# Performance work log

Measured on AMD Instinct MI355X. Metric: run time of the kernel, lower is better.

Reference implementation:

```python
import jax, jax.numpy as jnp
import numpy as np

# CODABlocks (codomain attention) with per_channel_attention=True:
# token_codimension = head_codimension = 1, scale = 2, n_modes = [32, 32],
# mixer_modes = [16, 16], temperature = 1.0, instance_norm (affine) everywhere.
N_HEADS = 16
TEMPERATURE = 1.0
EPS = 1e-5

def _gelu(z):
    return jax.nn.gelu(z, approximate=False)  # matches torch F.gelu default (erf)

def instance_norm(x, g, b):
    # x: (B, C, H, W); normalize over spatial dims per (sample, channel), affine.
    mu = jnp.mean(x, axis=(-2, -1), keepdims=True)
    var = jnp.var(x, axis=(-2, -1), keepdims=True)
    return (x - mu) * jax.lax.rsqrt(var + EPS) * g[:, None, None] + b[:, None, None]

def conv1x1(x, w, b):
    return jnp.einsum('bihw,io->bohw', x, w) + b[None, :, None, None]

def fourier_resample(x, out_shape):
    # FFT-based spatial resampling (mode truncation / zero-pad), norm='forward'.
    if tuple(x.shape[-2:]) == tuple(out_shape):
        return x
    Ho, Wo = out_shape
    xft = jnp.fft.rfftn(x, axes=(-2, -1), norm='forward')
    out = jnp.zeros(x.shape[:-2] + (Ho, Wo // 2 + 1), dtype=xft.dtype)
    hk = min(x.shape[-2], Ho) // 2
    wk = min(xft.shape[-1], Wo // 2 + 1)
    out = out.at[..., :hk, :wk].set(xft[..., :hk, :wk])
    out = out.at[..., -hk:, :wk].set(xft[..., -hk:, :wk])
    return jnp.fft.irfftn(out, s=out_shape, axes=(-2, -1), norm='forward')

def spectral_conv(x, w, out_shape):
    # Truncated-mode spectral convolution (dense weights, equiv. to tucker rank=1.0).
    # w: (Cin, Cout, 2*mh, mw, 2) -> complex weight on kept Fourier modes.
    wc = w[..., 0] + 1j * w[..., 1]
    mh = wc.shape[2] // 2
    mw = wc.shape[3]
    Ho, Wo = out_shape
    xft = jnp.fft.rfftn(x, axes=(-2, -1), norm='forward')   # (B, Cin, H, W//2+1)
    top = jnp.einsum('bihw,iohw->bohw', xft[:, :, :mh, :mw], wc[:, :, :mh])
    bot = jnp.einsum('bihw,iohw->bohw', xft[:, :, -mh:, :mw], wc[:, :, mh:])
    out_ft = jnp.zeros((x.shape[0], wc.shape[1], Ho, Wo // 2 + 1), dtype=xft.dtype)
    out_ft = out_ft.at[:, :, :mh, :mw].set(top)
    out_ft = out_ft.at[:, :, -mh:, :mw].set(bot)
    return jnp.fft.irfftn(out_ft, s=out_shape, axes=(-2, -1), norm='forward')

def fno_layer(x, spec_w, skip_w, skip_b, out_shape, norm=None, act=None):
    # One FNOBlocks layer: spectral conv + (resampled) linear skip, optional norm/act.
    xs = fourier_resample(conv1x1(x, skip_w, skip_b), out_shape)
    xf = spectral_conv(x, spec_w, out_shape)
    if norm is not None:
        xf = instance_norm(xf, *norm)
    y = xf + xs
    return act(y) if act is not None else y

def codano_forward(x, key_w, key_skip_w, key_skip_b, query_w, query_skip_w, query_skip_b, value_w, value_skip_w, value_skip_b, proj_w, proj_skip_w, proj_skip_b, norm1_g, norm1_b, attn_norm_g, attn_norm_b, norm2_g, norm2_b, mixer_w1, mixer_skip_w1, mixer_skip_b1, mixer_norm_g1, mixer_norm_b1, mixer_w2, mixer_skip_w2, mixer_skip_b2, mixer_norm_g2, mixer_norm_b2, mixer_out_g, mixer_out_b):
    b, t, H, W = x.shape   # token codim d = 1 -> channel dim == number of tokens
    tokens = x.reshape(b * t, 1, H, W)
    tokens_norm = instance_norm(tokens, norm1_g, norm1_b)
    Hs, Ws = H // 2, W // 2   # K, Q downsampled by scale = 2
    k = fno_layer(tokens_norm, key_w, key_skip_w, key_skip_b, (Hs, Ws))
    q = fno_layer(tokens_norm, query_w, query_skip_w, query_skip_b, (Hs, Ws))
    v = fno_layer(tokens_norm, value_w, value_skip_w, value_skip_b, (H, W))

    def heads_flat(z):
        hh, ww = z.shape[-2:]
        # (b*t, n_heads*d, h, w) -> (b, heads, t, d*h*w), d = 1
        return z.reshape(b, t, N_HEADS, hh * ww).transpose(0, 2, 1, 3)

    kf, qf, vf = heads_flat(k), heads_flat(q), heads_flat(v)
    scale = jnp.sqrt(jnp.asarray(kf.shape[-1], jnp.float32)) * TEMPERATURE
    dprod = jax.nn.softmax(jnp.einsum('bhtd,bhsd->bhts', qf, kf) / scale, axis=-1)
    attn = jnp.einsum('bhts,bhsd->bhtd', dprod, vf)      # (b, heads, t, H*W)
    attn = attn.transpose(0, 2, 1, 3).reshape(b * t, N_HEADS, H, W)
    # multi-head projection back to token codimension (n_heads -> 1)
    attn = fno_layer(attn, proj_w, proj_skip_w, proj_skip_b, (H, W))
    attn = instance_norm(attn + tokens, attn_norm_g, attn_norm_b)
    # permutation-equivariant mixer: 2 FNO layers shared across all tokens
    m = instance_norm(attn, norm2_g, norm2_b)
    m = fno_layer(m, mixer_w1, mixer_skip_w1, mixer_skip_b1, (H, W), norm=(mixer_norm_g1, mixer_norm_b1), act=_gelu)
    m = fno_layer(m, mixer_w2, mixer_skip_w2, mixer_skip_b2, (H, W), norm=(mixer_norm_g2, mixer_norm_b2))
    out = instance_norm(m, mixer_out_g, mixer_out_b) + attn
    return out.reshape(b, t, H, W)

def setup_inputs():
    key = jax.random.key(0)
    ks = list(jax.random.split(key, 32))
    f32 = jnp.float32
    def W_(k, shape, s=0.02):
        return (s * jax.random.normal(k, shape)).astype(f32)
    B, T, H, Wd = 4, 32, 128, 128
    mh_s, mw_s = 16, 9    # mixer_modes [16,16]: 2*(16//2) rows, 16//2+1 rfft cols
    mh_f, mw_f = 32, 17   # n_modes [32,32]
    return {
        'x': jax.random.normal(ks[0], (B, T, H, Wd), dtype=f32),
        'key_w': W_(ks[1], (1, N_HEADS, mh_s, mw_s, 2)),
        'key_skip_w': W_(ks[2], (1, N_HEADS), 0.5),
        'key_skip_b': W_(ks[3], (N_HEADS,)),
        'query_w': W_(ks[4], (1, N_HEADS, mh_s, mw_s, 2)),
        'query_skip_w': W_(ks[5], (1, N_HEADS), 0.5),
        'query_skip_b': W_(ks[6], (N_HEADS,)),
        'value_w': W_(ks[7], (1, N_HEADS, mh_s, mw_s, 2)),
        'value_skip_w': W_(ks[8], (1, N_HEADS), 0.5),
        'value_skip_b': W_(ks[9], (N_HEADS,)),
        'proj_w': W_(ks[10], (N_HEADS, 1, mh_f, mw_f, 2)),
        'proj_skip_w': W_(ks[11], (N_HEADS, 1), 0.25),
        'proj_skip_b': W_(ks[12], (1,)),
        'norm1_g': jnp.ones((1,), f32), 'norm1_b': jnp.zeros((1,), f32),
        'attn_norm_g': jnp.ones((1,), f32), 'attn_norm_b': jnp.zeros((1,), f32),
        'norm2_g': jnp.ones((1,), f32), 'norm2_b': jnp.zeros((1,), f32),
        'mixer_w1': W_(ks[13], (1, 1, mh_f, mw_f, 2)),
        'mixer_skip_w1': W_(ks[14], (1, 1), 0.5),
        'mixer_skip_b1': W_(ks[15], (1,)),
        'mixer_norm_g1': jnp.ones((1,), f32), 'mixer_norm_b1': jnp.zeros((1,), f32),
        'mixer_w2': W_(ks[16], (1, 1, mh_f, mw_f, 2)),
        'mixer_skip_w2': W_(ks[17], (1, 1), 0.5),
        'mixer_skip_b2': W_(ks[18], (1,)),
        'mixer_norm_g2': jnp.ones((1,), f32), 'mixer_norm_b2': jnp.zeros((1,), f32),
        'mixer_out_g': jnp.ones((1,), f32), 'mixer_out_b': jnp.zeros((1,), f32),
    }

def reference(x, key_w, key_skip_w, key_skip_b, query_w, query_skip_w, query_skip_b, value_w, value_skip_w, value_skip_b, proj_w, proj_skip_w, proj_skip_b, norm1_g, norm1_b, attn_norm_g, attn_norm_b, norm2_g, norm2_b, mixer_w1, mixer_skip_w1, mixer_skip_b1, mixer_norm_g1, mixer_norm_b1, mixer_w2, mixer_skip_w2, mixer_skip_b2, mixer_norm_g2, mixer_norm_b2, mixer_out_g, mixer_out_b):
    return codano_forward(x, key_w, key_skip_w, key_skip_b, query_w, query_skip_w, query_skip_b, value_w, value_skip_w, value_skip_b, proj_w, proj_skip_w, proj_skip_b, norm1_g, norm1_b, attn_norm_g, attn_norm_b, norm2_g, norm2_b, mixer_w1, mixer_skip_w1, mixer_skip_b1, mixer_norm_g1, mixer_norm_b1, mixer_w2, mixer_skip_w2, mixer_skip_b2, mixer_norm_g2, mixer_norm_b2, mixer_out_g, mixer_out_b)
```

## Files before the change

### kernel.cpp

```cpp
#include <hip/hip_runtime.h>
#include <cmath>

#define PI_F 3.14159265358979323846f
#define NTOK 128
#define NPIX 16384
#define NHEADS 16

__device__ __forceinline__ void block_reduce2(float& a, float& b){
  __shared__ float sa[4], sb[4];
  __syncthreads();
  for (int o=32;o>0;o>>=1){ a += __shfl_down(a,o); b += __shfl_down(b,o); }
  int w = threadIdx.x>>6, l = threadIdx.x&63;
  if (l==0){ sa[w]=a; sb[w]=b; }
  __syncthreads();
  a = sa[0]+sa[1]+sa[2]+sa[3];
  b = sb[0]+sb[1]+sb[2]+sb[3];
}

__device__ __forceinline__ float block_reduce1(float a){
  __shared__ float sa[4];
  __syncthreads();
  for (int o=32;o>0;o>>=1) a += __shfl_down(a,o);
  int w = threadIdx.x>>6, l = threadIdx.x&63;
  if (l==0) sa[w]=a;
  __syncthreads();
  return sa[0]+sa[1]+sa[2]+sa[3];
}

__device__ __forceinline__ float gelu_f(float y){
  return 0.5f*y*(1.f + erff(y*0.70710678118f));
}

__device__ __forceinline__ void affine_from(const float* __restrict__ ps, float g, float bb, int t,
                                            float& a, float& b0){
  float sum=0.f,sq=0.f;
  #pragma unroll
  for (int s=0;s<8;s++){ const float* p=ps+((size_t)t*8+s)*2; sum+=p[0]; sq+=p[1]; }
  const float iN=1.f/NPIX;
  float mu=sum*iN, var=sq*iN-mu*mu;
  a=rsqrtf(var+1e-5f)*g;
  b0=bb-mu*a;
}
__device__ __forceinline__ void scalA_from(const float* __restrict__ psA, float ag, float n2g, int t,
                                           float& muZ, float& aA, float& a0){
  float sum=0.f,sq=0.f;
  #pragma unroll
  for (int s=0;s<16;s++){ const float* p=psA+((size_t)t*16+s)*2; sum+=p[0]; sq+=p[1]; }
  const float iN=1.f/NPIX;
  muZ=sum*iN; float var=sq*iN-muZ*muZ;
  float inv=rsqrtf(var+1e-5f);
  aA=inv*ag;
  float var2=aA*aA*var;
  a0=aA*rsqrtf(var2+1e-5f)*n2g;
}
__device__ __forceinline__ void scalB_from(const float* __restrict__ psB, float mng1, int t,
                                           float& mu1, float& c1){
  float sum=0.f,sq=0.f;
  #pragma unroll
  for (int s=0;s<16;s++){ const float* p=psB+((size_t)t*16+s)*2; sum+=p[0]; sq+=p[1]; }
  const float iN=1.f/NPIX;
  mu1=sum*iN; float var=sq*iN-mu1*mu1;
  c1=rsqrtf(var+1e-5f)*mng1;
}
__device__ __forceinline__ void scalC_from(const float* __restrict__ psC, float mng2, float K, float sw,
                                           float outg, int t,
                                           float& mu2f, float& c2, float& mu3, float& c3){
  float sf=0.f,sfsq=0.f,sm=0.f,smsq=0.f,sx=0.f;
  #pragma unroll
  for (int s=0;s<16;s++){
    const float* p=psC+((size_t)t*16+s)*5;
    sf+=p[0]; sfsq+=p[1]; sm+=p[2]; smsq+=p[3]; sx+=p[4];
  }
  const float iN=1.f/NPIX;
  mu2f=sf*iN; float var2=sfsq*iN-mu2f*mu2f;
  c2=rsqrtf(var2+1e-5f)*mng2;
  float Em1=sm*iN, Em1sq=smsq*iN, Exm=sx*iN;
  float Em2=K+sw*Em1;
  float Em2sq = c2*c2*var2 + sw*sw*Em1sq + K*K
              + 2.f*c2*sw*(Exm - mu2f*Em1) + 2.f*K*sw*Em1;
  float var_m2=Em2sq-Em2*Em2;
  mu3=Em2;
  c3=rsqrtf(var_m2+1e-5f)*outg;
}

__global__ __launch_bounds__(256) void k_scol(const float* __restrict__ x,
                        float* __restrict__ A, float* __restrict__ pstat){
  int bx=blockIdx.x;
  if (bx<1024){
    __shared__ float rows[2048];
    __shared__ float S1[2592];
    __shared__ float tw[256];
    int base = bx*16;
    for (int i=threadIdx.x;i<2048;i+=256) rows[i] = x[(size_t)base*128 + i];
    for (int p=threadIdx.x;p<128;p+=256){ float sn,cs; sincosf(-(2.f*PI_F/128.f)*(float)p,&sn,&cs); tw[p*2]=cs; tw[p*2+1]=sn; }
    __syncthreads();
    for (int e=threadIdx.x;e<1280;e+=256){
      int r=e/80, q=e%80, w0=q/5, k=q%5;
      const float* y=rows+r*128+w0;
      float re=0.f, im=0.f;
      #pragma unroll
      for (int w1=0;w1<8;w1++){
        int p=(16*k*w1)&127;
        float v=y[w1*16];
        re+=v*tw[p*2]; im+=v*tw[p*2+1];
      }
      float* o=S1+r*162+q*2; o[0]=re; o[1]=im;
    }
    __syncthreads();
    for (int e=threadIdx.x;e<528;e+=256){
      int r=e/33, c=e%33;
      int m=c&7; int ks=m; float sg=1.f;
      if (m>4){ ks=8-m; sg=-1.f; }
      const float* Sp=S1+r*162+ks*2;
      float re=0.f, im=0.f;
      #pragma unroll
      for (int w0=0;w0<16;w0++){
        int p=(c*w0)&127;
        float cr=tw[p*2], ci=tw[p*2+1];
        float sr=Sp[w0*10], si=sg*Sp[w0*10+1];
        re += sr*cr - si*ci;
        im += sr*ci + si*cr;
      }
      float* o=A+((size_t)(base+r)*33+c)*2; o[0]=re; o[1]=im;
    }
  } else {
    int u=bx-1024; int t=u>>3, slab=u&7;
    const float* xs = x + (size_t)t*NPIX + slab*2048;
    float sum=0.f, sq=0.f;
    for (int i=threadIdx.x;i<2048;i+=256){ float v=xs[i]; sum+=v; sq+=v*v; }
    block_reduce2(sum,sq);
    if (threadIdx.x==0){ float* o=pstat+((size_t)t*8+slab)*2; o[0]=sum; o[1]=sq; }
  }
}

__global__ __launch_bounds__(256) void k_rowfft64(const float* __restrict__ A,
                          const float* __restrict__ pstat0,
                          const float* __restrict__ n1g, const float* __restrict__ n1b,
                          float* __restrict__ X64, float* __restrict__ X64h){
  int s=blockIdx.x, cg2=blockIdx.y;
  int c0=cg2*11;
  __shared__ float a[128*11*2];
  __shared__ float S1[11*290];
  __shared__ float S[64][11][2];
  __shared__ float tw[128][2];
  for (int i=threadIdx.x;i<128*22;i+=256){
    int r=i/22, q=i%22;
    a[(r*11+(q>>1))*2+(q&1)] = A[((size_t)(s*128+r)*33 + c0)*2 + q];
  }
  for (int p=threadIdx.x;p<128;p+=256){ float sn,cs; sincosf(-(2.f*PI_F/128.f)*(float)p,&sn,&cs); tw[p][0]=cs; tw[p][1]=sn; }
  float af,b0; affine_from(pstat0, n1g[0], n1b[0], s, af, b0);
  __syncthreads();
  for (int e=threadIdx.x;e<1408;e+=256){
    int cl=e>>7, q=e&127, h0=q>>3, k=q&7;
    float re=0.f, im=0.f;
    #pragma unroll
    for (int h1=0;h1<8;h1++){
      int p=(16*k*h1)&127;
      float cr=tw[p][0], ci=tw[p][1];
      const float* ap=a+((h0+16*h1)*11+cl)*2;
      float ar=ap[0], ai=ap[1];
      re += ar*cr - ai*ci;
      im += ar*ci + ai*cr;
    }
    float* o=S1+cl*290+h0*18+k*2; o[0]=re; o[1]=im;
  }
  __syncthreads();
  const float sc=1.f/16384.f;
  for (int e=threadIdx.x;e<64*11;e+=256){
    int i2=e/11, cl=e%11;
    int r=(i2<32)? i2 : i2+64;
    int k=r&7;
    const float* Sp=S1+cl*290+k*2;
    float re=0.f, im=0.f;
    #pragma unroll
    for (int h0=0;h0<16;h0++){
      int p=(r*h0)&127;
      float cr=tw[p][0], ci=tw[p][1];
      float sr=Sp[h0*18], si=Sp[h0*18+1];
      re += sr*cr - si*ci;
      im += sr*ci + si*cr;
    }
    float vr = af*re*sc, vi = af*im*sc;
    if (r==0 && (c0+cl)==0) vr += b0;
    S[i2][cl][0]=vr; S[i2][cl][1]=vi;
  }
  __syncthreads();
  for (int e=threadIdx.x;e<64*11;e+=256){
    int r=e/11, cl=e%11; int c=c0+cl;
    float vr=S[r][cl][0], vi=S[r][cl][1];
    float* o=X64+((size_t)s*(64*33)+r*33+c)*2; o[0]=vr; o[1]=vi;
    float hr=vr, hi=vi;
    if (c==0 || c==32){
      int pr=(64-r)&63;
      hr=0.5f*(vr+S[pr][cl][0]);
      hi=0.5f*(vi-S[pr][cl][1]);
    }
    float* oh=X64h+((size_t)s*(64*33)+r*33+c)*2; oh[0]=hr; oh[1]=hi;
  }
}

__global__ __launch_bounds__(256) void k_UeZYw(const float* __restrict__ X64, const float* __restrict__ X64h,
    const float* __restrict__ qw, const float* __restrict__ qsw,
    const float* __restrict__ kw, const float* __restrict__ ksw,
    const float* __restrict__ value_w, const float* __restrict__ vsw, const float* __restrict__ vsb,
    const float* __restrict__ proj_w, const float* __restrict__ psw,
    float* __restrict__ Zq, float* __restrict__ Zk, float* __restrict__ Yw,
    float* __restrict__ Ue){
  __shared__ float sh[4224];
  int bx=blockIdx.x;
  if (bx<2048){
    int t=bx>>4, h=bx&15;
    float* Xs = sh;
    float2* xh0 = (float2*)(sh+1092);
    for (int e=threadIdx.x;e<544;e+=256){
      int j=e/17, c=e%17;
      int i2=(j<16)? j : (j+32);
      const float* xp = X64 + ((size_t)t*(64*33) + i2*33 + c)*2;
      Xs[e*2]=xp[0]; Xs[e*2+1]=xp[1];
    }
    if (threadIdx.x<17){
      int j=threadIdx.x;
      int r=(j<=8)? j : j+47;
      const float* hp = X64h + ((size_t)t*(64*33) + r*33)*2;
      xh0[j]=make_float2(hp[0],hp[1]);
    }
    __syncthreads();
    float aq=qsw[h], ak=ksw[h];
    for (int e=threadIdx.x;e<306;e+=256){
      int side=e/153, m=e%153;
      int j=m/9, c=m%9;
      int jj=(j<=8)? j : j+15;
      const float* W = side? kw : qw;
      float a = side? ak : aq;
      float prx=0.f, pry=0.f;
      if (j!=8){
        int jw=(j<8)? j : j-1;
        const float* wp = W + ((size_t)(h*16+jw)*9 + c)*2;
        float xrr=Xs[(jj*17+c)*2], xri=Xs[(jj*17+c)*2+1];
        prx = wp[0]*xrr - wp[1]*xri;
        pry = wp[0]*xri + wp[1]*xrr;
      }
      float Vx=prx, Vy=pry;
      if (c==0){
        int jp = (j==0)? 0 : 17-j;
        float ppx=0.f, ppy=0.f;
        if (jp!=8){
          int jw2=(jp<8)? jp : jp-1;
          const float* wp2 = W + ((size_t)(h*16+jw2)*9)*2;
          int jj2=(jp<=8)? jp : jp+15;
          float x2r=Xs[(jj2*17)*2], x2i=Xs[(jj2*17)*2+1];
          ppx = wp2[0]*x2r - wp2[1]*x2i;
          ppy = wp2[0]*x2i + wp2[1]*x2r;
        }
        Vx = 0.5f*(prx + ppx);
        Vy = 0.5f*(pry - ppy);
      }
      float xmr, xmi;
      if (c==0){ xmr=xh0[j].x; xmi=xh0[j].y; }
      else { xmr=Xs[(jj*17+c)*2]; xmi=Xs[(jj*17+c)*2+1]; }
      float zr = a*xmr + Vx;
      float zi = a*xmi + Vy;
      float wf = (side && c!=0)? 2.f : 1.f;
      float* dst = (side? Zk : Zq) + ((size_t)(t*16+h))*306 + m*2;
      dst[0]=wf*zr; dst[1]=wf*zi;
    }
    int b=t>>5, s=t&31;
    float vw=vsw[h], vb=vsb[h], pw=psw[h];
    size_t obase = ((size_t)(b*16+h)*32 + s)*1088;
    for (int e=threadIdx.x;e<544;e+=256){
      int j=e/17, c=e%17;
      float xr=Xs[e*2], xi=Xs[e*2+1];
      float wvr=0.f,wvi=0.f;
      if (c<=8 && (j<8||j>=24)){
        int jw=(j<8)? j : (j-16);
        const float* wv = value_w + ((size_t)(h*16+jw)*9 + c)*2;
        wvr=wv[0]; wvi=wv[1];
      }
      float Mr=xr*wvr-xi*wvi, Mi=xr*wvi+xi*wvr;
      float Mhr=Mr, Mhi=Mi;
      if (c==0){
        float Pr2=0.f,Pi2=0.f;
        int jp2=(j==0)?0:((j==16)?-1:32-j);
        if (jp2>=0 && (jp2<8||jp2>=24)){
          int jw2=(jp2<8)? jp2 : (jp2-16);
          const float* wv2=value_w+((size_t)(h*16+jw2)*9)*2;
          float pxr=Xs[(jp2*17)*2], pxi=Xs[(jp2*17)*2+1];
          Pr2=pxr*wv2[0]-pxi*wv2[1];
          Pi2=pxr*wv2[1]+pxi*wv2[0];
        }
        Mhr=0.5f*(Mr+Pr2); Mhi=0.5f*(Mi-Pi2);
      }
      float Yr=vw*xr+Mhr+((e==0)? vb:0.f);
      float Yi=vw*xi+Mhi;
      const float* pc=proj_w+((size_t)(h*32+j)*17+c)*2;
      float pr=pc[0], pi=pc[1];
      float* o=Yw+obase+e*2;
      o[0]=pr*Yr-pi*Yi+pw*Mr;
      o[1]=pr*Yi+pi*Yr+pw*Mi;
    }
  } else {
    int u=bx-2048;
    int b=u>>8, rem=u&255, t=rem>>3, sg=rem&7;
    float2* xt=(float2*)sh;
    const float2* src = (const float2*)(X64h + ((size_t)(b*32+t))*4224);
    for (int m=threadIdx.x;m<2112;m+=256){
      int r=m/33, c=m%33;
      bool excl = (c<=8) && (r<=8 || r>=56);
      float w = excl? 0.f : ((c==0||c==32)? 1.f : 2.f);
      float2 v = src[m];
      xt[m]=make_float2(v.x*w, v.y*w);
    }
    __syncthreads();
    float acc[4]={0.f,0.f,0.f,0.f};
    const float2* s0=(const float2*)(X64h + ((size_t)(b*32+sg*4))*4224);
    for (int m=threadIdx.x;m<2112;m+=256){
      float2 a2=xt[m];
      #pragma unroll
      for (int j=0;j<4;j++){
        float2 b2=s0[(size_t)j*2112+m];
        acc[j]+=a2.x*b2.x+a2.y*b2.y;
      }
    }
    for (int j=0;j<4;j++){
      float r=block_reduce1(acc[j]);
      if (threadIdx.x==0) Ue[((size_t)(b*32+t))*32 + sg*4+j]=r;
    }
  }
}

__global__ __launch_bounds__(256) void k_scores2(const float* __restrict__ Zq, const float* __restrict__ Zk,
                          const float* __restrict__ Ue,
                          const float* __restrict__ qsw, const float* __restrict__ qsb,
                          const float* __restrict__ ksw, const float* __restrict__ ksb,
                          float* __restrict__ P){
  int b=blockIdx.x, h=blockIdx.y, tz=blockIdx.z;
  __shared__ float2 zq[16][154];
  __shared__ float2 zk[16][154];
  __shared__ float Pl[16][33];
  for (int i=threadIdx.x;i<16*153;i+=256){
    int t=i/153, m=i%153;
    zq[t][m]=((const float2*)(Zq + ((size_t)((b*32+tz*16+t)*16+h))*306))[m];
  }
  float aq=qsw[h], ak=ksw[h], bq=qsb[h], bk=ksb[h];
  float aqak=aq*ak;
  int tl=threadIdx.x>>4, sl=threadIdx.x&15;
  for (int ch=0; ch<2; ch++){
    __syncthreads();
    for (int i=threadIdx.x;i<16*153;i+=256){
      int s=i/153, m=i%153;
      zk[s][m]=((const float2*)(Zk + ((size_t)((b*32+ch*16+s)*16+h))*306))[m];
    }
    __syncthreads();
    float acc=0.f;
    for (int m=0;m<153;m++){
      float2 a2=zq[tl][m], c2=zk[sl][m];
      acc += a2.x*c2.x + a2.y*c2.y;
    }
    int s=ch*16+sl;
    float G = aqak*Ue[((size_t)(b*32+tz*16+tl))*32+s] + acc;
    Pl[tl][s] = 64.f*(G + bk*zq[tl][0].x + bq*zk[sl][0].x + bq*bk);
  }
  __syncthreads();
  if (threadIdx.x<16){
    int tt=threadIdx.x;
    float mx=-INFINITY;
    for (int s=0;s<32;s++) mx=fmaxf(mx,Pl[tt][s]);
    float e[32]; float sum=0.f;
    for (int s=0;s<32;s++){ e[s]=expf(Pl[tt][s]-mx); sum+=e[s]; }
    float inv=1.f/sum;
    size_t base=((size_t)(b*16+h)*32+tz*16+tt)*32;
    for (int s=0;s<32;s++) P[base+s]=e[s]*inv;
  }
}

__global__ __launch_bounds__(256) void k_SfSk(const float* __restrict__ x, const float* __restrict__ P,
        const float* __restrict__ Yw,
        const float* __restrict__ pw, const float* __restrict__ vw,
        const float* __restrict__ pstat0, const float* __restrict__ n1g, const float* __restrict__ n1b,
        float* __restrict__ Sfp, float* __restrict__ sk){
  __shared__ float sh[4096];
  int bx=blockIdx.x;
  if (bx<272){
    int b=bx/68, rem=bx%68, ec=rem/4, g=rem%4;
    int e0=ec*64, hs0=g*128;
    float (*Pl)[32] = (float(*)[32])sh;
    for (int i=threadIdx.x;i<128*32;i+=256){
      int hsl=i>>5, t=i&31;
      int hs=hs0+hsl, h=hs>>5, s=hs&31;
      Pl[hsl][t]=P[(((size_t)(b*16+h)*32)+t)*32+s];
    }
    __syncthreads();
    int el=threadIdx.x&63, tg=threadIdx.x>>6;
    float acc[8];
    #pragma unroll
    for (int j=0;j<8;j++) acc[j]=0.f;
    const float* Yb = Yw + ((size_t)b*512 + hs0)*1088 + e0 + el;
    #pragma unroll 4
    for (int hsl=0;hsl<128;hsl++){
      float y = Yb[(size_t)hsl*1088];
      #pragma unroll
      for (int j=0;j<8;j++) acc[j] += Pl[hsl][tg*8+j]*y;
    }
    #pragma unroll
    for (int j=0;j<8;j++){
      int t=tg*8+j;
      Sfp[((size_t)(b*32+t)*4+g)*1088 + e0 + el] = acc[j];
    }
  } else {
    int u=bx-272;
    int b=u>>6, rem=u&63, ch=rem>>1, tt=rem&1;
    int pxb=ch*512;
    float* Rs = sh;
    float* cbs = sh+512;
    float* as2 = sh+528;
    float* b0s = sh+560;
    if (threadIdx.x<32){
      float a,b0; affine_from(pstat0, n1g[0], n1b[0], b*32+threadIdx.x, a, b0);
      as2[threadIdx.x]=a; b0s[threadIdx.x]=b0;
    }
    __syncthreads();
    for (int rr=threadIdx.x; rr<512; rr+=256){
      int tl=rr>>5, s=rr&31;
      int t=tt*16+tl;
      float acc=0.f;
      for (int h=0;h<16;h++)
        acc += pw[h]*vw[h]*P[(((size_t)(b*16+h)*32)+t)*32+s];
      Rs[tl*32+s]=acc*as2[s];
      float cb=acc*b0s[s];
      for (int o=16;o>0;o>>=1) cb+=__shfl_down(cb,o,32);
      if (s==0) cbs[tl]=cb;
    }
    __syncthreads();
    float a0[16], a1[16];
    #pragma unroll
    for (int t=0;t<16;t++){ a0[t]=0.f; a1[t]=0.f; }
    for (int s=0;s<32;s++){
      const float* xp = x + ((size_t)(b*32+s))*NPIX + pxb;
      float v0=xp[threadIdx.x], v1=xp[threadIdx.x+256];
      #pragma unroll
      for (int t=0;t<16;t++){ float r=Rs[t*32+s]; a0[t]+=r*v0; a1[t]+=r*v1; }
    }
    #pragma unroll
    for (int t=0;t<16;t++){
      int gt=tt*16+t;
      float cb=cbs[t];
      float* op = sk + ((size_t)(b*32+gt))*NPIX + pxb;
      op[threadIdx.x]=a0[t]+cb; op[threadIdx.x+256]=a1[t]+cb;
    }
  }
}

__global__ __launch_bounds__(256) void k_f0sp(const float* __restrict__ Sfp,
        const float* __restrict__ sk, const float* __restrict__ x,
        const float* __restrict__ P, const float* __restrict__ X64,
        const float* __restrict__ pstat0,
        const float* __restrict__ n1g, const float* __restrict__ n1b,
        const float* __restrict__ pw, const float* __restrict__ vw,
        const float* __restrict__ psw, const float* __restrict__ vsb, const float* __restrict__ psb,
        float* __restrict__ zf, float* __restrict__ pstatA, float* __restrict__ sp){
  __shared__ float sh[1616];
  int bx=blockIdx.x;
  if (bx<2048){
    int bt=bx>>4, slab=bx&15;
    float* Ss=sh; float* T=sh+1088; float* tw=sh+1360;
    for (int i=threadIdx.x;i<1088;i+=256){
      const float* sp4 = Sfp + (size_t)bt*4352 + i;
      Ss[i] = sp4[0]+sp4[1088]+sp4[2176]+sp4[3264];
    }
    for (int p=threadIdx.x;p<128;p+=256){ float sn,cs; sincosf((2.f*PI_F/128.f)*(float)p,&sn,&cs); tw[p*2]=cs; tw[p*2+1]=sn; }
    __syncthreads();
    int h0 = slab*8;
    for (int e=threadIdx.x;e<136;e+=256){
      int hl=e/17, c=e%17; int h=h0+hl;
      float re=0.f, im=0.f;
      for (int j=0;j<32;j++){
        int r=(j<16)? j : (j+96);
        int p=(r*h)&127;
        float cs=tw[p*2], sn=tw[p*2+1];
        float ar=Ss[(j*17+c)*2], ai=Ss[(j*17+c)*2+1];
        re += ar*cs - ai*sn;
        im += ar*sn + ai*cs;
      }
      T[e*2]=re; T[e*2+1]=im;
    }
    __syncthreads();
    size_t base = (size_t)bt*NPIX + h0*128;
    float Cb = psb[0];
    for (int hh=0;hh<16;hh++) Cb += psw[hh]*vsb[hh];
    int w=threadIdx.x&127, hl0=threadIdx.x>>7;
    float cw[16], swt[16];
    #pragma unroll
    for (int c=0;c<16;c++){ int p=((c+1)*w)&127; cw[c]=tw[p*2]; swt[c]=tw[p*2+1]; }
    float sum=0.f, sq=0.f;
    #pragma unroll
    for (int pp=0;pp<4;pp++){
      int hl=hl0+2*pp;
      const float2* Th=(const float2*)(T+hl*34);
      float v=Th[0].x;
      #pragma unroll
      for (int c=0;c<16;c++){ float2 th=Th[c+1]; v += 2.f*(th.x*cw[c] - th.y*swt[c]); }
      int pos=hl*128+w;
      float val = v + sk[base+pos] + x[base+pos] + Cb;
      zf[base+pos]=val; sum+=val; sq+=val*val;
    }
    block_reduce2(sum,sq);
    if (threadIdx.x==0){ float* o=pstatA+((size_t)bt*16+slab)*2; o[0]=sum; o[1]=sq; }
  } else {
    int u=bx-2048;
    int bt=u>>1, ec=u&1; int b=bt>>5, t=bt&31;
    float* Sfl=sh; float* Rs=sh+1088;
    if (threadIdx.x<32){
      int s=threadIdx.x; float acc=0.f;
      for (int h=0;h<16;h++)
        acc += pw[h]*vw[h]*P[(((size_t)(b*16+h)*32)+t)*32+s];
      Rs[s]=acc;
    }
    for (int i=threadIdx.x;i<1088;i+=256){
      const float* sp4 = Sfp + (size_t)bt*4352 + i;
      Sfl[i]=sp4[0]+sp4[1088]+sp4[2176]+sp4[3264];
    }
    __syncthreads();
    float a_t,b0_t; affine_from(pstat0,n1g[0],n1b[0],bt,a_t,b0_t);
    float Cb=psb[0];
    for (int h=0;h<16;h++) Cb+=psw[h]*vsb[h];
    float inva=1.f/a_t;
    int e1=ec*272, e2=e1+272;
    for (int e=e1+threadIdx.x;e<e2;e+=256){
      int j=e/17, c=e%17;
      float sr=Sfl[e*2], si=Sfl[e*2+1];
      if (c==0){
        if (j==0){ si=0.f; }
        else if (j==16){ sr*=0.5f; si*=0.5f; }
        else { int jp=32-j; sr=0.5f*(sr+Sfl[jp*34]); si=0.5f*(si-Sfl[jp*34+1]); }
      }
      int i2=(j<16)? j : (j+32);
      float re=0.f, im=0.f;
      const float* xb = X64 + ((size_t)(b*32)*(64*33) + i2*33 + c)*2;
      for (int s=0;s<32;s++){
        const float* xp = xb + (size_t)s*(64*33)*2;
        float r=Rs[s];
        re += r*xp[0]; im += r*xp[1];
      }
      const float* xt = X64 + ((size_t)bt*(64*33) + i2*33 + c)*2;
      re += inva*xt[0]; im += inva*xt[1];
      float zr=sr+re, zi=si+im;
      if (e==0) zr += Cb - b0_t*inva;
      sp[((size_t)bt*544+e)*2]=zr; sp[((size_t)bt*544+e)*2+1]=zi;
    }
  }
}

__global__ __launch_bounds__(256) void k_field1(const float* __restrict__ sp, const float* __restrict__ wm,
        const float* __restrict__ pstatA,
        const float* __restrict__ ag, const float* __restrict__ n2g, const float* __restrict__ n2b,
        float* __restrict__ fd1, float* __restrict__ pstatB){
  int bt = blockIdx.x, slab = blockIdx.y;
  __shared__ float Ss[1088];
  __shared__ float T[8*17*2];
  __shared__ float tw[128][2];
  float muZ,aA,a0;
  scalA_from(pstatA, ag[0], n2g[0], bt, muZ, aA, a0);
  float d0 = n2b[0] - muZ*a0;
  for (int e=threadIdx.x;e<544;e+=256){
    float xr=a0*sp[((size_t)bt*544+e)*2] + ((e==0)? d0 : 0.f);
    float xi=a0*sp[((size_t)bt*544+e)*2+1];
    float wr=wm[e*2], wi=wm[e*2+1];
    Ss[e*2]=xr*wr-xi*wi; Ss[e*2+1]=xr*wi+xi*wr;
  }
  for (int p=threadIdx.x;p<128;p+=256){ float sn,cs; sincosf((2.f*PI_F/128.f)*(float)p,&sn,&cs); tw[p][0]=cs; tw[p][1]=sn; }
  __syncthreads();
  int h0 = slab*8;
  for (int e=threadIdx.x;e<8*17;e+=256){
    int hl=e/17, c=e%17; int h=h0+hl;
    float re=0.f, im=0.f;
    for (int j=0;j<32;j++){
      int r=(j<16)? j : (j+96);
      int p=(r*h)&127;
      float cs=tw[p][0], sn=tw[p][1];
      float ar=Ss[(j*17+c)*2], ai=Ss[(j*17+c)*2+1];
      re += ar*cs - ai*sn;
      im += ar*sn + ai*cs;
    }
    T[e*2]=re; T[e*2+1]=im;
  }
  __syncthreads();
  size_t base = (size_t)bt*NPIX + h0*128;
  int w=threadIdx.x&127, hl0=threadIdx.x>>7;
  float cw[16], swt[16];
  #pragma unroll
  for (int c=0;c<16;c++){ int p=((c+1)*w)&127; cw[c]=tw[p][0]; swt[c]=tw[p][1]; }
  float sum=0.f, sq=0.f;
  #pragma unroll
  for (int pp=0;pp<4;pp++){
    int hl=hl0+2*pp;
    const float2* Th=(const float2*)(T+hl*34);
    float v=Th[0].x;
    #pragma unroll
    for (int c=0;c<16;c++){ float2 th=Th[c+1]; v += 2.f*(th.x*cw[c] - th.y*swt[c]); }
    int pos=hl*128+w;
    fd1[base+pos]=v; sum+=v; sq+=v*v;
  }
  block_reduce2(sum,sq);
  if (threadIdx.x==0){ float* o=pstatB+((size_t)bt*16+slab)*2; o[0]=sum; o[1]=sq; }
}

__global__ __launch_bounds__(256) void k_colA1(const float* __restrict__ f1, const float* __restrict__ z,
        const float* __restrict__ pstatA, const float* __restrict__ pstatB,
        const float* __restrict__ ag, const float* __restrict__ n2g, const float* __restrict__ mng1,
        const float* __restrict__ n2b,
        const float* __restrict__ mnb1, const float* __restrict__ msw1, const float* __restrict__ msb1,
        float* __restrict__ A){
  __shared__ float rows[16*128];
  __shared__ float S1[2592];
  __shared__ float tw[128][2];
  int grow = blockIdx.x*16;
  int t = grow>>7;
  float muZ,aA,a0;
  scalA_from(pstatA, ag[0], n2g[0], t, muZ, aA, a0);
  float b2 = n2b[0];
  float mu1,c1;
  scalB_from(pstatB, mng1[0], t, mu1, c1);
  float nb=mnb1[0], sw=msw1[0], sb=msb1[0];
  for (int i=threadIdx.x;i<2048;i+=256){
    size_t gi=(size_t)grow*128+i;
    float m0v=(z[gi]-muZ)*a0+b2;
    float y=(f1[gi]-mu1)*c1+nb + m0v*sw + sb;
    rows[i]=gelu_f(y);
  }
  for (int p=threadIdx.x;p<128;p+=256){ float sn,cs; sincosf(-(2.f*PI_F/128.f)*(float)p,&sn,&cs); tw[p][0]=cs; tw[p][1]=sn; }
  __syncthreads();
  for (int e=threadIdx.x;e<1280;e+=256){
    int r=e/80, q=e%80, w0=q/5, k=q%5;
    const float* y=rows+r*128+w0;
    float re=0.f, im=0.f;
    #pragma unroll
    for (int w1=0;w1<8;w1++){
      int p=(16*k*w1)&127;
      float v=y[w1*16];
      re+=v*tw[p][0]; im+=v*tw[p][1];
    }
    float* o=S1+r*162+q*2; o[0]=re; o[1]=im;
  }
  __syncthreads();
  for (int e=threadIdx.x;e<272;e+=256){
    int r=e/17, c=e%17;
    int m=c&7; int ks=m; float sg=1.f;
    if (m>4){ ks=8-m; sg=-1.f; }
    const float* Sp=S1+r*162+ks*2;
    float re=0.f, im=0.f;
    #pragma unroll
    for (int w0=0;w0<16;w0++){
      int p=(c*w0)&127;
      float cr=tw[p][0], ci=tw[p][1];
      float sr=Sp[w0*10], si=sg*Sp[w0*10+1];
      re += sr*cr - si*ci;
      im += sr*ci + si*cr;
    }
    float* o=A+((size_t)(grow+r)*17+c)*2; o[0]=re; o[1]=im;
  }
}

__global__ __launch_bounds__(256) void k_rowfft32(const float* __restrict__ A, float* __restrict__ spec){
  int s=blockIdx.x, cg2=blockIdx.y;
  int c0 = (cg2==0)? 0 : (1+cg2*4);
  int nc = (cg2==0)? 5 : 4;
  __shared__ float a[128*5*2];
  __shared__ float S1[5*290];
  __shared__ float tw[128][2];
  for (int i=threadIdx.x;i<128*nc*2;i+=256){
    int r=i/(2*nc), q=i%(2*nc);
    a[(r*5+(q>>1))*2+(q&1)] = A[((size_t)(s*128+r)*17 + c0)*2 + q];
  }
  for (int p=threadIdx.x;p<128;p+=256){ float sn,cs; sincosf(-(2.f*PI_F/128.f)*(float)p,&sn,&cs); tw[p][0]=cs; tw[p][1]=sn; }
  __syncthreads();
  for (int e=threadIdx.x;e<nc*128;e+=256){
    int cl=e>>7, q=e&127, h0=q>>3, k=q&7;
    float re=0.f, im=0.f;
    #pragma unroll
    for (int h1=0;h1<8;h1++){
      int p=(16*k*h1)&127;
      float cr=tw[p][0], ci=tw[p][1];
      const float* ap=a+((h0+16*h1)*5+cl)*2;
      float ar=ap[0], ai=ap[1];
      re += ar*cr - ai*ci;
      im += ar*ci + ai*cr;
    }
    float* o=S1+cl*290+h0*18+k*2; o[0]=re; o[1]=im;
  }
  __syncthreads();
  const float sc=1.f/16384.f;
  for (int e=threadIdx.x;e<32*nc;e+=256){
    int j=e/nc, cl=e%nc;
    int r=(j<16)? j : (j+96);
    int k=r&7;
    const float* Sp=S1+cl*290+k*2;
    float re=0.f,im=0.f;
    #pragma unroll
    for (int h0=0;h0<16;h0++){
      int p=(r*h0)&127;
      float cr=tw[p][0], ci=tw[p][1];
      float sr=Sp[h0*18], si=Sp[h0*18+1];
      re += sr*cr - si*ci;
      im += sr*ci + si*cr;
    }
    float* o=spec+((size_t)s*544 + j*17 + c0+cl)*2;
    o[0]=re*sc; o[1]=im*sc;
  }
}

__global__ __launch_bounds__(256) void k_field2(const float* __restrict__ sp2, const float* __restrict__ wm,
        const float* __restrict__ f1, const float* __restrict__ z,
        const float* __restrict__ pstatA, const float* __restrict__ pstatB,
        const float* __restrict__ ag, const float* __restrict__ n2g, const float* __restrict__ mng1,
        const float* __restrict__ n2b, const float* __restrict__ mnb1,
        const float* __restrict__ msw1, const float* __restrict__ msb1,
        float* __restrict__ fd2, float* __restrict__ pstatC){
  int bt = blockIdx.x, slab = blockIdx.y;
  __shared__ float Ss[1088];
  __shared__ float T[8*17*2];
  __shared__ float tw[128][2];
  for (int e=threadIdx.x;e<544;e+=256){
    float xr=sp2[((size_t)bt*544+e)*2], xi=sp2[((size_t)bt*544+e)*2+1];
    float wr=wm[e*2], wi=wm[e*2+1];
    Ss[e*2]=xr*wr-xi*wi; Ss[e*2+1]=xr*wi+xi*wr;
  }
  for (int p=threadIdx.x;p<128;p+=256){ float sn,cs; sincosf((2.f*PI_F/128.f)*(float)p,&sn,&cs); tw[p][0]=cs; tw[p][1]=sn; }
  __syncthreads();
  int h0 = slab*8;
  for (int e=threadIdx.x;e<8*17;e+=256){
    int hl=e/17, c=e%17; int h=h0+hl;
    float re=0.f, im=0.f;
    for (int j=0;j<32;j++){
      int r=(j<16)? j : (j+96);
      int p=(r*h)&127;
      float cs=tw[p][0], sn=tw[p][1];
      float ar=Ss[(j*17+c)*2], ai=Ss[(j*17+c)*2+1];
      re += ar*cs - ai*sn;
      im += ar*sn + ai*cs;
    }
    T[e*2]=re; T[e*2+1]=im;
  }
  __syncthreads();
  size_t base = (size_t)bt*NPIX + h0*128;
  float muZ,aA,a0,mu1,c1;
  scalA_from(pstatA, ag[0], n2g[0], bt, muZ, aA, a0);
  scalB_from(pstatB, mng1[0], bt, mu1, c1);
  float b2=n2b[0], nb1=mnb1[0], sw1=msw1[0], sb1=msb1[0];
  int w=threadIdx.x&127, hl0=threadIdx.x>>7;
  float cw[16], swt[16];
  #pragma unroll
  for (int c=0;c<16;c++){ int p=((c+1)*w)&127; cw[c]=tw[p][0]; swt[c]=tw[p][1]; }
  float s_f=0.f,s_fsq=0.f,s_m=0.f,s_msq=0.f,s_x=0.f;
  #pragma unroll
  for (int pp=0;pp<4;pp++){
    int hl=hl0+2*pp;
    const float2* Th=(const float2*)(T+hl*34);
    float v=Th[0].x;
    #pragma unroll
    for (int c=0;c<16;c++){ float2 th=Th[c+1]; v += 2.f*(th.x*cw[c] - th.y*swt[c]); }
    int pos=hl*128+w;
    size_t gi=base+pos;
    float m0v=(z[gi]-muZ)*a0+b2;
    float y=(f1[gi]-mu1)*c1+nb1 + m0v*sw1 + sb1;
    float m1v=gelu_f(y);
    fd2[gi]=v;
    s_f+=v; s_fsq+=v*v; s_m+=m1v; s_msq+=m1v*m1v; s_x+=v*m1v;
  }
  block_reduce2(s_f,s_fsq);
  block_reduce2(s_m,s_msq);
  s_x = block_reduce1(s_x);
  if (threadIdx.x==0){
    float* o=pstatC+((size_t)bt*16+slab)*5;
    o[0]=s_f; o[1]=s_fsq; o[2]=s_m; o[3]=s_msq; o[4]=s_x;
  }
}

__global__ __launch_bounds__(256) void k_final2(const float* __restrict__ z, const float* __restrict__ f1,
        const float* __restrict__ f2,
        const float* __restrict__ pstatA, const float* __restrict__ pstatB, const float* __restrict__ pstatC,
        const float* __restrict__ ag, const float* __restrict__ n2g, const float* __restrict__ mng1,
        const float* __restrict__ mng2, const float* __restrict__ outg,
        const float* __restrict__ ab, const float* __restrict__ n2b,
        const float* __restrict__ mnb1, const float* __restrict__ msw1, const float* __restrict__ msb1,
        const float* __restrict__ mnb2, const float* __restrict__ msw2, const float* __restrict__ msb2,
        const float* __restrict__ outb, float* __restrict__ out){
  int bt=blockIdx.x, slab=blockIdx.y;
  float muZ,aA,a0,mu1,c1,mu2f,c2,mu3,c3;
  scalA_from(pstatA, ag[0], n2g[0], bt, muZ, aA, a0);
  scalB_from(pstatB, mng1[0], bt, mu1, c1);
  float sw2=msw2[0], K=mnb2[0]+msb2[0];
  scalC_from(pstatC, mng2[0], K, sw2, outg[0], bt, mu2f, c2, mu3, c3);
  float b1=ab[0], b2=n2b[0], nb1=mnb1[0], sw1=msw1[0], sb1=msb1[0];
  float nb2=mnb2[0], sb2=msb2[0], bo=outb[0];
  size_t base=(size_t)bt*NPIX + (size_t)slab*1024;
  for (int i=threadIdx.x;i<1024;i+=256){
    size_t gi=base+i;
    float zv=z[gi];
    float m0v=(zv-muZ)*a0+b2;
    float a2v=(zv-muZ)*aA+b1;
    float y=(f1[gi]-mu1)*c1+nb1 + m0v*sw1 + sb1;
    float m1v=gelu_f(y);
    float m2v=(f2[gi]-mu2f)*c2+nb2 + m1v*sw2 + sb2;
    out[gi]=(m2v-mu3)*c3+bo+a2v;
  }
}

extern "C" void kernel_launch(void* const* d_in, const int* in_sizes, int n_in,
                              void* d_out, int out_size, void* d_ws, size_t ws_size,
                              hipStream_t stream){
  const float* x        = (const float*)d_in[0];
  const float* key_w    = (const float*)d_in[1];
  const float* key_sw   = (const float*)d_in[2];
  const float* key_sb   = (const float*)d_in[3];
  const float* query_w  = (const float*)d_in[4];
  const float* query_sw = (const float*)d_in[5];
  const float* query_sb = (const float*)d_in[6];
  const float* value_w  = (const float*)d_in[7];
  const float* value_sw = (const float*)d_in[8];
  const float* value_sb = (const float*)d_in[9];
  const float* proj_w   = (const float*)d_in[10];
  const float* proj_sw  = (const float*)d_in[11];
  const float* proj_sb  = (const float*)d_in[12];
  const float* norm1_g  = (const float*)d_in[13];
  const float* norm1_b  = (const float*)d_in[14];
  const float* attn_g   = (const float*)d_in[15];
  const float* attn_b   = (const float*)d_in[16];
  const float* norm2_g  = (const float*)d_in[17];
  const float* norm2_b  = (const float*)d_in[18];
  const float* mw1      = (const float*)d_in[19];
  const float* msw1     = (const float*)d_in[20];
  const float* msb1     = (const float*)d_in[21];
  const float* mng1     = (const float*)d_in[22];
  const float* mnb1     = (const float*)d_in[23];
  const float* mw2      = (const float*)d_in[24];
  const float* msw2     = (const float*)d_in[25];
  const float* msb2     = (const float*)d_in[26];
  const float* mng2     = (const float*)d_in[27];
  const float* mnb2     = (const float*)d_in[28];
  const float* outg     = (const float*)d_in[29];
  const float* outb     = (const float*)d_in[30];
  float* out = (float*)d_out;
  float* ws  = (float*)d_ws;

  size_t off=0;
  float* A   = ws + off; off += (size_t)128*128*33*2;
  float* X64 = ws + off; off += (size_t)128*64*33*2;
  float* X64h= ws + off; off += (size_t)128*64*33*2;
  float* Zq  = ws + off; off += (size_t)128*16*306;
  float* Zk  = ws + off; off += (size_t)128*16*306;
  float* Ue  = ws + off; off += (size_t)4*32*32;
  float* P   = ws + off; off += (size_t)4*16*32*32;
  float* Yw  = ws + off; off += (size_t)2048*1088;
  float* Sfp = ws + off; off += (size_t)128*4*1088;
  float* sk  = ws + off; off += (size_t)128*16384;
  float* zf  = ws + off; off += (size_t)128*16384;
  float* fd1 = ws + off; off += (size_t)128*16384;
  float* fd2 = ws + off; off += (size_t)128*16384;
  float* sp  = ws + off; off += (size_t)128*544*2;
  float* sp2 = ws + off; off += (size_t)128*544*2;
  float* pstat0 = ws + off; off += (size_t)128*8*2;
  float* pstatA = ws + off; off += (size_t)128*16*2;
  float* pstatB = ws + off; off += (size_t)128*16*2;
  float* pstatC = ws + off; off += (size_t)128*16*5;

  k_scol<<<2048,256,0,stream>>>(x, A, pstat0);
  k_rowfft64<<<dim3(128,3),256,0,stream>>>(A, pstat0, norm1_g, norm1_b, X64, X64h);
  k_UeZYw<<<3072,256,0,stream>>>(X64, X64h, query_w, query_sw, key_w, key_sw,
      value_w, value_sw, value_sb, proj_w, proj_sw, Zq, Zk, Yw, Ue);
  k_scores2<<<dim3(4,16,2),256,0,stream>>>(Zq, Zk, Ue, query_sw, query_sb, key_sw, key_sb, P);
  k_SfSk<<<528,256,0,stream>>>(x, P, Yw, proj_sw, value_sw, pstat0, norm1_g, norm1_b, Sfp, sk);
  k_f0sp<<<2304,256,0,stream>>>(Sfp, sk, x, P, X64, pstat0, norm1_g, norm1_b,
      proj_sw, value_sw, proj_sw, value_sb, proj_sb, zf, pstatA, sp);
  k_field1<<<dim3(128,16),256,0,stream>>>(sp, mw1, pstatA, attn_g, norm2_g, norm2_b, fd1, pstatB);
  k_colA1<<<1024,256,0,stream>>>(fd1, zf, pstatA, pstatB, attn_g, norm2_g, mng1,
      norm2_b, mnb1, msw1, msb1, A);
  k_rowfft32<<<dim3(128,4),256,0,stream>>>(A, sp2);
  k_field2<<<dim3(128,16),256,0,stream>>>(sp2, mw2, fd1, zf, pstatA, pstatB,
      attn_g, norm2_g, mng1, norm2_b, mnb1, msw1, msb1, fd2, pstatC);
  k_final2<<<dim3(128,16),256,0,stream>>>(zf, fd1, fd2, pstatA, pstatB, pstatC,
      attn_g, norm2_g, mng1, mng2, outg, attn_b, norm2_b,
      mnb1, msw1, msb1, mnb2, msw2, msb2, outb, out);
}
```

Before: 271.7 us.

## Fuse all stages into one persistent megakernel with grid-wide barriers

Turns each of the eleven kernels into device functions and runs them inside one persistent kernel of 1024 blocks, separated by atomic-counter grid barriers. This removes per-kernel launch overhead and the drain/fill gaps between dependent stages. The occupancy query guards against deadlock by falling back to the old multi-kernel path. The score stage also changes its key chunking from 2x16 to 4x8, leaving half the threads idle in the dot-product loop. The cost is that barrier spinning and stages with fewer blocks than the grid leave part of the machine idle, plus the loss of __restrict__ hints.

```diff
diff --git a/kernel.cpp b/kernel.cpp
--- a/kernel.cpp
+++ b/kernel.cpp
@@ -5,6 +5,7 @@
 #define NTOK 128
 #define NPIX 16384
 #define NHEADS 16
+#define NBLK 1024u
 
 __device__ __forceinline__ void block_reduce2(float& a, float& b){
   __shared__ float sa[4], sb[4];
@@ -31,7 +32,19 @@
   return 0.5f*y*(1.f + erff(y*0.70710678118f));
 }
 
-__device__ __forceinline__ void affine_from(const float* __restrict__ ps, float g, float bb, int t,
+__device__ __forceinline__ void gbar(unsigned* cnt){
+  __syncthreads();
+  __threadfence();
+  if (threadIdx.x==0){
+    atomicAdd(cnt, 1u);
+    while (__hip_atomic_load(cnt, __ATOMIC_RELAXED, __HIP_MEMORY_SCOPE_AGENT) < NBLK)
+      __builtin_amdgcn_s_sleep(2);
+  }
+  __syncthreads();
+  __threadfence();
+}
+
+__device__ __forceinline__ void affine_from(const float* ps, float g, float bb, int t,
                                             float& a, float& b0){
   float sum=0.f,sq=0.f;
   #pragma unroll
@@ -41,7 +54,7 @@
   a=rsqrtf(var+1e-5f)*g;
   b0=bb-mu*a;
 }
-__device__ __forceinline__ void scalA_from(const float* __restrict__ psA, float ag, float n2g, int t,
+__device__ __forceinline__ void scalA_from(const float* psA, float ag, float n2g, int t,
                                            float& muZ, float& aA, float& a0){
   float sum=0.f,sq=0.f;
   #pragma unroll
@@ -53,7 +66,7 @@
   float var2=aA*aA*var;
   a0=aA*rsqrtf(var2+1e-5f)*n2g;
 }
-__device__ __forceinline__ void scalB_from(const float* __restrict__ psB, float mng1, int t,
+__device__ __forceinline__ void scalB_from(const float* psB, float mng1, int t,
                                            float& mu1, float& c1){
   float sum=0.f,sq=0.f;
   #pragma unroll
@@ -62,7 +75,7 @@
   mu1=sum*iN; float var=sq*iN-mu1*mu1;
   c1=rsqrtf(var+1e-5f)*mng1;
 }
-__device__ __forceinline__ void scalC_from(const float* __restrict__ psC, float mng2, float K, float sw,
+__device__ __forceinline__ void scalC_from(const float* psC, float mng2, float K, float sw,
                                            float outg, int t,
                                            float& mu2f, float& c2, float& mu3, float& c3){
   float sf=0.f,sfsq=0.f,sm=0.f,smsq=0.f,sx=0.f;
@@ -83,16 +96,14 @@
   c3=rsqrtf(var_m2+1e-5f)*outg;
 }
 
-__global__ __launch_bounds__(256) void k_scol(const float* __restrict__ x,
-                        float* __restrict__ A, float* __restrict__ pstat){
-  int bx=blockIdx.x;
+
+__device__ __forceinline__ void st_scol(int bx, float* sh, const float* x,
+                                        float* A, float* pstat){
   if (bx<1024){
-    __shared__ float rows[2048];
-    __shared__ float S1[2592];
-    __shared__ float tw[256];
+    float* rows=sh; float* S1=sh+2048; float* tw=sh+4640;
     int base = bx*16;
     for (int i=threadIdx.x;i<2048;i+=256) rows[i] = x[(size_t)base*128 + i];
-    for (int p=threadIdx.x;p<128;p+=256){ float sn,cs; sincosf(-(2.f*PI_F/128.f)*(float)p,&sn,&cs); tw[p*2]=cs; tw[p*2+1]=sn; }
+    for (int q=threadIdx.x;q<128;q+=256){ float sn,cs; sincosf(-(2.f*PI_F/128.f)*(float)q,&sn,&cs); tw[q*2]=cs; tw[q*2+1]=sn; }
     __syncthreads();
     for (int e=threadIdx.x;e<1280;e+=256){
       int r=e/80, q=e%80, w0=q/5, k=q%5;
@@ -133,21 +144,20 @@
   }
 }
 
-__global__ __launch_bounds__(256) void k_rowfft64(const float* __restrict__ A,
-                          const float* __restrict__ pstat0,
-                          const float* __restrict__ n1g, const float* __restrict__ n1b,
-                          float* __restrict__ X64, float* __restrict__ X64h){
-  int s=blockIdx.x, cg2=blockIdx.y;
+__device__ __forceinline__ void st_row64(int u, float* sh, const float* A,
+                          const float* pstat0, const float* n1g, const float* n1b,
+                          float* X64, float* X64h){
+  int s=u%128, cg2=u/128;
   int c0=cg2*11;
-  __shared__ float a[128*11*2];
-  __shared__ float S1[11*290];
-  __shared__ float S[64][11][2];
-  __shared__ float tw[128][2];
+  float* a=sh;
+  float* S1=sh+2816;
+  float* S=sh+6006;
+  float* tw=sh+7414;
   for (int i=threadIdx.x;i<128*22;i+=256){
     int r=i/22, q=i%22;
     a[(r*11+(q>>1))*2+(q&1)] = A[((size_t)(s*128+r)*33 + c0)*2 + q];
   }
-  for (int p=threadIdx.x;p<128;p+=256){ float sn,cs; sincosf(-(2.f*PI_F/128.f)*(float)p,&sn,&cs); tw[p][0]=cs; tw[p][1]=sn; }
+  for (int q=threadIdx.x;q<128;q+=256){ float sn,cs; sincosf(-(2.f*PI_F/128.f)*(float)q,&sn,&cs); tw[q*2]=cs; tw[q*2+1]=sn; }
   float af,b0; affine_from(pstat0, n1g[0], n1b[0], s, af, b0);
   __syncthreads();
   for (int e=threadIdx.x;e<1408;e+=256){
@@ -156,7 +166,7 @@
     #pragma unroll
     for (int h1=0;h1<8;h1++){
       int p=(16*k*h1)&127;
-      float cr=tw[p][0], ci=tw[p][1];
+      float cr=tw[p*2], ci=tw[p*2+1];
       const float* ap=a+((h0+16*h1)*11+cl)*2;
       float ar=ap[0], ai=ap[1];
       re += ar*cr - ai*ci;
@@ -175,39 +185,35 @@
     #pragma unroll
     for (int h0=0;h0<16;h0++){
       int p=(r*h0)&127;
-      float cr=tw[p][0], ci=tw[p][1];
+      float cr=tw[p*2], ci=tw[p*2+1];
       float sr=Sp[h0*18], si=Sp[h0*18+1];
       re += sr*cr - si*ci;
       im += sr*ci + si*cr;
     }
     float vr = af*re*sc, vi = af*im*sc;
     if (r==0 && (c0+cl)==0) vr += b0;
-    S[i2][cl][0]=vr; S[i2][cl][1]=vi;
+    S[(i2*11+cl)*2]=vr; S[(i2*11+cl)*2+1]=vi;
   }
   __syncthreads();
   for (int e=threadIdx.x;e<64*11;e+=256){
     int r=e/11, cl=e%11; int c=c0+cl;
-    float vr=S[r][cl][0], vi=S[r][cl][1];
+    float vr=S[(r*11+cl)*2], vi=S[(r*11+cl)*2+1];
     float* o=X64+((size_t)s*(64*33)+r*33+c)*2; o[0]=vr; o[1]=vi;
     float hr=vr, hi=vi;
     if (c==0 || c==32){
       int pr=(64-r)&63;
-      hr=0.5f*(vr+S[pr][cl][0]);
-      hi=0.5f*(vi-S[pr][cl][1]);
+      hr=0.5f*(vr+S[(pr*11+cl)*2]);
+      hi=0.5f*(vi-S[(pr*11+cl)*2+1]);
     }
     float* oh=X64h+((size_t)s*(64*33)+r*33+c)*2; oh[0]=hr; oh[1]=hi;
   }
 }
 
-__global__ __launch_bounds__(256) void k_UeZYw(const float* __restrict__ X64, const float* __restrict__ X64h,
-    const float* __restrict__ qw, const float* __restrict__ qsw,
-    const float* __restrict__ kw, const float* __restrict__ ksw,
-    const float* __restrict__ value_w, const float* __restrict__ vsw, const float* __restrict__ vsb,
-    const float* __restrict__ proj_w, const float* __restrict__ psw,
-    float* __restrict__ Zq, float* __restrict__ Zk, float* __restrict__ Yw,
-    float* __restrict__ Ue){
-  __shared__ float sh[4224];
-  int bx=blockIdx.x;
+__device__ __forceinline__ void st_uezyw(int bx, float* sh, const float* X64, const float* X64h,
+    const float* qw, const float* qsw, const float* kw, const float* ksw,
+    const float* value_w, const float* vsw, const float* vsb,
+    const float* proj_w, const float* psw,
+    float* Zq, float* Zk, float* Yw, float* Ue){
   if (bx<2048){
     int t=bx>>4, h=bx&15;
     float* Xs = sh;
@@ -265,7 +271,7 @@
       dst[0]=wf*zr; dst[1]=wf*zi;
     }
     int b=t>>5, s=t&31;
-    float vw=vsw[h], vb=vsb[h], pw=psw[h];
+    float vw_=vsw[h], vb=vsb[h], pw=psw[h];
     size_t obase = ((size_t)(b*16+h)*32 + s)*1088;
     for (int e=threadIdx.x;e<544;e+=256){
       int j=e/17, c=e%17;
@@ -290,8 +296,8 @@
         }
         Mhr=0.5f*(Mr+Pr2); Mhi=0.5f*(Mi-Pi2);
       }
-      float Yr=vw*xr+Mhr+((e==0)? vb:0.f);
-      float Yi=vw*xi+Mhi;
+      float Yr=vw_*xr+Mhr+((e==0)? vb:0.f);
+      float Yi=vw_*xi+Mhi;
       const float* pc=proj_w+((size_t)(h*32+j)*17+c)*2;
       float pr=pc[0], pi=pc[1];
       float* o=Yw+obase+e*2;
@@ -328,58 +334,55 @@
   }
 }
 
-__global__ __launch_bounds__(256) void k_scores2(const float* __restrict__ Zq, const float* __restrict__ Zk,
-                          const float* __restrict__ Ue,
-                          const float* __restrict__ qsw, const float* __restrict__ qsb,
-                          const float* __restrict__ ksw, const float* __restrict__ ksb,
-                          float* __restrict__ P){
-  int b=blockIdx.x, h=blockIdx.y, tz=blockIdx.z;
-  __shared__ float2 zq[16][154];
-  __shared__ float2 zk[16][154];
-  __shared__ float Pl[16][33];
+__device__ __forceinline__ void st_scores(int u, float* sh, const float* Zq, const float* Zk,
+                          const float* Ue, const float* qsw, const float* qsb,
+                          const float* ksw, const float* ksb, float* P){
+  int b=u&3, h=(u>>2)&15, tz=u>>6;
+  float2* zq=(float2*)sh;
+  float2* zk=(float2*)(sh+4928);
+  float*  Pl=sh+7392;
   for (int i=threadIdx.x;i<16*153;i+=256){
     int t=i/153, m=i%153;
-    zq[t][m]=((const float2*)(Zq + ((size_t)((b*32+tz*16+t)*16+h))*306))[m];
+    zq[t*154+m]=((const float2*)(Zq + ((size_t)((b*32+tz*16+t)*16+h))*306))[m];
   }
   float aq=qsw[h], ak=ksw[h], bq=qsb[h], bk=ksb[h];
   float aqak=aq*ak;
   int tl=threadIdx.x>>4, sl=threadIdx.x&15;
-  for (int ch=0; ch<2; ch++){
-    __syncthreads();
-    for (int i=threadIdx.x;i<16*153;i+=256){
+  for (int ch=0; ch<4; ch++){
+    __syncthreads();
+    for (int i=threadIdx.x;i<8*153;i+=256){
       int s=i/153, m=i%153;
-      zk[s][m]=((const float2*)(Zk + ((size_t)((b*32+ch*16+s)*16+h))*306))[m];
-    }
-    __syncthreads();
-    float acc=0.f;
-    for (int m=0;m<153;m++){
-      float2 a2=zq[tl][m], c2=zk[sl][m];
-      acc += a2.x*c2.x + a2.y*c2.y;
-    }
-    int s=ch*16+sl;
-    float G = aqak*Ue[((size_t)(b*32+tz*16+tl))*32+s] + acc;
-    Pl[tl][s] = 64.f*(G + bk*zq[tl][0].x + bq*zk[sl][0].x + bq*bk);
+      zk[s*154+m]=((const float2*)(Zk + ((size_t)((b*32+ch*8+s)*16+h))*306))[m];
+    }
+    __syncthreads();
+    if (sl<8){
+      float acc=0.f;
+      for (int m=0;m<153;m++){
+        float2 a2=zq[tl*154+m], c2=zk[sl*154+m];
+        acc += a2.x*c2.x + a2.y*c2.y;
+      }
+      int s=ch*8+sl;
+      float G = aqak*Ue[((size_t)(b*32+tz*16+tl))*32+s] + acc;
+      Pl[tl*32+s] = 64.f*(G + bk*zq[tl*154].x + bq*zk[sl*154].x + bq*bk);
+    }
   }
   __syncthreads();
   if (threadIdx.x<16){
     int tt=threadIdx.x;
     float mx=-INFINITY;
-    for (int s=0;s<32;s++) mx=fmaxf(mx,Pl[tt][s]);
+    for (int s=0;s<32;s++) mx=fmaxf(mx,Pl[tt*32+s]);
     float e[32]; float sum=0.f;
-    for (int s=0;s<32;s++){ e[s]=expf(Pl[tt][s]-mx); sum+=e[s]; }
+    for (int s=0;s<32;s++){ e[s]=expf(Pl[tt*32+s]-mx); sum+=e[s]; }
     float inv=1.f/sum;
     size_t base=((size_t)(b*16+h)*32+tz*16+tt)*32;
     for (int s=0;s<32;s++) P[base+s]=e[s]*inv;
   }
 }
 
-__global__ __launch_bounds__(256) void k_SfSk(const float* __restrict__ x, const float* __restrict__ P,
-        const float* __restrict__ Yw,
-        const float* __restrict__ pw, const float* __restrict__ vw,
-        const float* __restrict__ pstat0, const float* __restrict__ n1g, const float* __restrict__ n1b,
-        float* __restrict__ Sfp, float* __restrict__ sk){
-  __shared__ float sh[4096];
-  int bx=blockIdx.x;
+__device__ __forceinline__ void st_sfsk(int bx, float* sh, const float* x, const float* P,
+        const float* Yw, const float* pw, const float* vw,
+        const float* pstat0, const float* n1g, const float* n1b,
+        float* Sfp, float* sk){
   if (bx<272){
     int b=bx/68, rem=bx%68, ec=rem/4, g=rem%4;
     int e0=ec*64, hs0=g*128;
@@ -450,16 +453,12 @@
   }
 }
 
-__global__ __launch_bounds__(256) void k_f0sp(const float* __restrict__ Sfp,
-        const float* __restrict__ sk, const float* __restrict__ x,
-        const float* __restrict__ P, const float* __restrict__ X64,
-        const float* __restrict__ pstat0,
-        const float* __restrict__ n1g, const float* __restrict__ n1b,
-        const float* __restrict__ pw, const float* __restrict__ vw,
-        const float* __restrict__ psw, const float* __restrict__ vsb, const float* __restrict__ psb,
-        float* __restrict__ zf, float* __restrict__ pstatA, float* __restrict__ sp){
-  __shared__ float sh[1616];
-  int bx=blockIdx.x;
+__device__ __forceinline__ void st_f0sp(int bx, float* sh, const float* Sfp,
+        const float* sk, const float* x, const float* P, const float* X64,
+        const float* pstat0, const float* n1g, const float* n1b,
+        const float* pw, const float* vw,
+        const float* psw, const float* vsb, const float* psb,
+        float* zf, float* pstatA, float* sp){
   if (bx<2048){
     int bt=bx>>4, slab=bx&15;
     float* Ss=sh; float* T=sh+1088; float* tw=sh+1360;
@@ -467,7 +466,7 @@
       const float* sp4 = Sfp + (size_t)bt*4352 + i;
       Ss[i] = sp4[0]+sp4[1088]+sp4[2176]+sp4[3264];
     }
-    for (int p=threadIdx.x;p<128;p+=256){ float sn,cs; sincosf((2.f*PI_F/128.f)*(float)p,&sn,&cs); tw[p*2]=cs; tw[p*2+1]=sn; }
+    for (int q=threadIdx.x;q<128;q+=256){ float sn,cs; sincosf((2.f*PI_F/128.f)*(float)q,&sn,&cs); tw[q*2]=cs; tw[q*2+1]=sn; }
     __syncthreads();
     int h0 = slab*8;
     for (int e=threadIdx.x;e<136;e+=256){
@@ -550,14 +549,11 @@
   }
 }
 
-__global__ __launch_bounds__(256) void k_field1(const float* __restrict__ sp, const float* __restrict__ wm,
-        const float* __restrict__ pstatA,
-        const float* __restrict__ ag, const float* __restrict__ n2g, const float* __restrict__ n2b,
-        float* __restrict__ fd1, float* __restrict__ pstatB){
-  int bt = blockIdx.x, slab = blockIdx.y;
-  __shared__ float Ss[1088];
-  __shared__ float T[8*17*2];
-  __shared__ float tw[128][2];
+__device__ __forceinline__ void st_field1(int u, float* sh, const float* sp, const float* wm,
+        const float* pstatA, const float* ag, const float* n2g, const float* n2b,
+        float* fd1, float* pstatB){
+  int bt=u&127, slab=u>>7;
+  float* Ss=sh; float* T=sh+1088; float* tw=sh+1360;
   float muZ,aA,a0;
   scalA_from(pstatA, ag[0], n2g[0], bt, muZ, aA, a0);
   float d0 = n2b[0] - muZ*a0;
@@ -567,7 +563,7 @@
     float wr=wm[e*2], wi=wm[e*2+1];
     Ss[e*2]=xr*wr-xi*wi; Ss[e*2+1]=xr*wi+xi*wr;
   }
-  for (int p=threadIdx.x;p<128;p+=256){ float sn,cs; sincosf((2.f*PI_F/128.f)*(float)p,&sn,&cs); tw[p][0]=cs; tw[p][1]=sn; }
+  for (int q=threadIdx.x;q<128;q+=256){ float sn,cs; sincosf((2.f*PI_F/128.f)*(float)q,&sn,&cs); tw[q*2]=cs; tw[q*2+1]=sn; }
   __syncthreads();
   int h0 = slab*8;
   for (int e=threadIdx.x;e<8*17;e+=256){
@@ -576,7 +572,7 @@
     for (int j=0;j<32;j++){
       int r=(j<16)? j : (j+96);
       int p=(r*h)&127;
-      float cs=tw[p][0], sn=tw[p][1];
+      float cs=tw[p*2], sn=tw[p*2+1];
       float ar=Ss[(j*17+c)*2], ai=Ss[(j*17+c)*2+1];
       re += ar*cs - ai*sn;
       im += ar*sn + ai*cs;
@@ -588,7 +584,7 @@
   int w=threadIdx.x&127, hl0=threadIdx.x>>7;
   float cw[16], swt[16];
   #pragma unroll
-  for (int c=0;c<16;c++){ int p=((c+1)*w)&127; cw[c]=tw[p][0]; swt[c]=tw[p][1]; }
+  for (int c=0;c<16;c++){ int p=((c+1)*w)&127; cw[c]=tw[p*2]; swt[c]=tw[p*2+1]; }
   float sum=0.f, sq=0.f;
   #pragma unroll
   for (int pp=0;pp<4;pp++){
@@ -604,16 +600,12 @@
   if (threadIdx.x==0){ float* o=pstatB+((size_t)bt*16+slab)*2; o[0]=sum; o[1]=sq; }
 }
 
-__global__ __launch_bounds__(256) void k_colA1(const float* __restrict__ f1, const float* __restrict__ z,
-        const float* __restrict__ pstatA, const float* __restrict__ pstatB,
-        const float* __restrict__ ag, const float* __restrict__ n2g, const float* __restrict__ mng1,
-        const float* __restrict__ n2b,
-        const float* __restrict__ mnb1, const float* __restrict__ msw1, const float* __restrict__ msb1,
-        float* __restrict__ A){
-  __shared__ float rows[16*128];
-  __shared__ float S1[2592];
-  __shared__ float tw[128][2];
-  int grow = blockIdx.x*16;
+__device__ __forceinline__ void st_colA1(int u, float* sh, const float* f1, const float* z,
+        const float* pstatA, const float* pstatB,
+        const float* ag, const float* n2g, const float* mng1, const float* n2b,
+        const float* mnb1, const float* msw1, const float* msb1, float* A){
+  float* rows=sh; float* S1=sh+2048; float* tw=sh+4640;
+  int grow = u*16;
   int t = grow>>7;
   float muZ,aA,a0;
   scalA_from(pstatA, ag[0], n2g[0], t, muZ, aA, a0);
@@ -627,7 +619,7 @@
     float y=(f1[gi]-mu1)*c1+nb + m0v*sw + sb;
     rows[i]=gelu_f(y);
   }
-  for (int p=threadIdx.x;p<128;p+=256){ float sn,cs; sincosf(-(2.f*PI_F/128.f)*(float)p,&sn,&cs); tw[p][0]=cs; tw[p][1]=sn; }
+  for (int q=threadIdx.x;q<128;q+=256){ float sn,cs; sincosf(-(2.f*PI_F/128.f)*(float)q,&sn,&cs); tw[q*2]=cs; tw[q*2+1]=sn; }
   __syncthreads();
   for (int e=threadIdx.x;e<1280;e+=256){
     int r=e/80, q=e%80, w0=q/5, k=q%5;
@@ -637,7 +629,7 @@
     for (int w1=0;w1<8;w1++){
       int p=(16*k*w1)&127;
       float v=y[w1*16];
-      re+=v*tw[p][0]; im+=v*tw[p][1];
+      re+=v*tw[p*2]; im+=v*tw[p*2+1];
     }
     float* o=S1+r*162+q*2; o[0]=re; o[1]=im;
   }
@@ -651,7 +643,7 @@
     #pragma unroll
     for (int w0=0;w0<16;w0++){
       int p=(c*w0)&127;
-      float cr=tw[p][0], ci=tw[p][1];
+      float cr=tw[p*2], ci=tw[p*2+1];
       float sr=Sp[w0*10], si=sg*Sp[w0*10+1];
       re += sr*cr - si*ci;
       im += sr*ci + si*cr;
@@ -660,18 +652,18 @@
   }
 }
 
-__global__ __launch_bounds__(256) void k_rowfft32(const float* __restrict__ A, float* __restrict__ spec){
-  int s=blockIdx.x, cg2=blockIdx.y;
+__device__ __forceinline__ void st_row32(int u, float* sh, const float* A, float* spec){
+  int s=u&127, cg2=u>>7;
   int c0 = (cg2==0)? 0 : (1+cg2*4);
   int nc = (cg2==0)? 5 : 4;
-  __shared__ float a[128*5*2];
-  __shared__ float S1[5*290];
-  __shared__ float tw[128][2];
+  float* a=sh;
+  float* S1=sh+1280;
+  float* tw=sh+2730;
   for (int i=threadIdx.x;i<128*nc*2;i+=256){
     int r=i/(2*nc), q=i%(2*nc);
     a[(r*5+(q>>1))*2+(q&1)] = A[((size_t)(s*128+r)*17 + c0)*2 + q];
   }
-  for (int p=threadIdx.x;p<128;p+=256){ float sn,cs; sincosf(-(2.f*PI_F/128.f)*(float)p,&sn,&cs); tw[p][0]=cs; tw[p][1]=sn; }
+  for (int q=threadIdx.x;q<128;q+=256){ float sn,cs; sincosf(-(2.f*PI_F/128.f)*(float)q,&sn,&cs); tw[q*2]=cs; tw[q*2+1]=sn; }
   __syncthreads();
   for (int e=threadIdx.x;e<nc*128;e+=256){
     int cl=e>>7, q=e&127, h0=q>>3, k=q&7;
@@ -679,7 +671,7 @@
     #pragma unroll
     for (int h1=0;h1<8;h1++){
       int p=(16*k*h1)&127;
-      float cr=tw[p][0], ci=tw[p][1];
+      float cr=tw[p*2], ci=tw[p*2+1];
       const float* ap=a+((h0+16*h1)*5+cl)*2;
       float ar=ap[0], ai=ap[1];
       re += ar*cr - ai*ci;
@@ -698,7 +690,7 @@
     #pragma unroll
     for (int h0=0;h0<16;h0++){
       int p=(r*h0)&127;
-      float cr=tw[p][0], ci=tw[p][1];
+      float cr=tw[p*2], ci=tw[p*2+1];
       float sr=Sp[h0*18], si=Sp[h0*18+1];
       re += sr*cr - si*ci;
       im += sr*ci + si*cr;
@@ -708,23 +700,19 @@
   }
 }
 
-__global__ __launch_bounds__(256) void k_field2(const float* __restrict__ sp2, const float* __restrict__ wm,
-        const float* __restrict__ f1, const float* __restrict__ z,
-        const float* __restrict__ pstatA, const float* __restrict__ pstatB,
-        const float* __restrict__ ag, const float* __restrict__ n2g, const float* __restrict__ mng1,
-        const float* __restrict__ n2b, const float* __restrict__ mnb1,
-        const float* __restrict__ msw1, const float* __restrict__ msb1,
-        float* __restrict__ fd2, float* __restrict__ pstatC){
-  int bt = blockIdx.x, slab = blockIdx.y;
-  __shared__ float Ss[1088];
-  __shared__ float T[8*17*2];
-  __shared__ float tw[128][2];
+__device__ __forceinline__ void st_field2(int u, float* sh, const float* sp2, const float* wm,
+        const float* f1, const float* z, const float* pstatA, const float* pstatB,
+        const float* ag, const float* n2g, const float* mng1, const float* n2b,
+        const float* mnb1, const float* msw1, const float* msb1,
+        float* fd2, float* pstatC){
+  int bt=u&127, slab=u>>7;
+  float* Ss=sh; float* T=sh+1088; float* tw=sh+1360;
   for (int e=threadIdx.x;e<544;e+=256){
     float xr=sp2[((size_t)bt*544+e)*2], xi=sp2[((size_t)bt*544+e)*2+1];
     float wr=wm[e*2], wi=wm[e*2+1];
     Ss[e*2]=xr*wr-xi*wi; Ss[e*2+1]=xr*wi+xi*wr;
   }
-  for (int p=threadIdx.x;p<128;p+=256){ float sn,cs; sincosf((2.f*PI_F/128.f)*(float)p,&sn,&cs); tw[p][0]=cs; tw[p][1]=sn; }
+  for (int q=threadIdx.x;q<128;q+=256){ float sn,cs; sincosf((2.f*PI_F/128.f)*(float)q,&sn,&cs); tw[q*2]=cs; tw[q*2+1]=sn; }
   __syncthreads();
   int h0 = slab*8;
   for (int e=threadIdx.x;e<8*17;e+=256){
@@ -733,7 +721,7 @@
     for (int j=0;j<32;j++){
       int r=(j<16)? j : (j+96);
       int p=(r*h)&127;
-      float cs=tw[p][0], sn=tw[p][1];
+      float cs=tw[p*2], sn=tw[p*2+1];
       float ar=Ss[(j*17+c)*2], ai=Ss[(j*17+c)*2+1];
       re += ar*cs - ai*sn;
       im += ar*sn + ai*cs;
@@ -749,7 +737,7 @@
   int w=threadIdx.x&127, hl0=threadIdx.x>>7;
   float cw[16], swt[16];
   #pragma unroll
-  for (int c=0;c<16;c++){ int p=((c+1)*w)&127; cw[c]=tw[p][0]; swt[c]=tw[p][1]; }
+  for (int c=0;c<16;c++){ int p=((c+1)*w)&127; cw[c]=tw[p*2]; swt[c]=tw[p*2+1]; }
   float s_f=0.f,s_fsq=0.f,s_m=0.f,s_msq=0.f,s_x=0.f;
   #pragma unroll
   for (int pp=0;pp<4;pp++){
@@ -775,16 +763,12 @@
   }
 }
 
-__global__ __launch_bounds__(256) void k_final2(const float* __restrict__ z, const float* __restrict__ f1,
-        const float* __restrict__ f2,
-        const float* __restrict__ pstatA, const float* __restrict__ pstatB, const float* __restrict__ pstatC,
-        const float* __restrict__ ag, const float* __restrict__ n2g, const float* __restrict__ mng1,
-        const float* __restrict__ mng2, const float* __restrict__ outg,
-        const float* __restrict__ ab, const float* __restrict__ n2b,
-        const float* __restrict__ mnb1, const float* __restrict__ msw1, const float* __restrict__ msb1,
-        const float* __restrict__ mnb2, const float* __restrict__ msw2, const float* __restrict__ msb2,
-        const float* __restrict__ outb, float* __restrict__ out){
-  int bt=blockIdx.x, slab=blockIdx.y;
+__device__ __forceinline__ void st_final(int u, const float* z, const float* f1, const float* f2,
+        const float* pstatA, const float* pstatB, const float* pstatC,
+        const float* ag, const float* n2g, const float* mng1, const float* mng2, const float* outg,
+        const float* ab, const float* n2b, const float* mnb1, const float* msw1, const float* msb1,
+        const float* mnb2, const float* msw2, const float* msb2, const float* outb, float* out){
+  int bt=u&127, slab=u>>7;
   float muZ,aA,a0,mu1,c1,mu2f,c2,mu3,c3;
   scalA_from(pstatA, ag[0], n2g[0], bt, muZ, aA, a0);
   scalB_from(pstatB, mng1[0], bt, mu1, c1);
@@ -803,6 +787,111 @@
     float m2v=(f2[gi]-mu2f)*c2+nb2 + m1v*sw2 + sb2;
     out[gi]=(m2v-mu3)*c3+bo+a2v;
   }
+}
+
+struct MP {
+  const float *x,*key_w,*key_sw,*key_sb,*query_w,*query_sw,*query_sb,
+    *value_w,*value_sw,*value_sb,*proj_w,*proj_sw,*proj_sb,
+    *norm1_g,*norm1_b,*attn_g,*attn_b,*norm2_g,*norm2_b,
+    *mw1,*msw1,*msb1,*mng1,*mnb1,*mw2,*msw2,*msb2,*mng2,*mnb2,*outg,*outb;
+  float *A,*X64,*X64h,*Zq,*Zk,*Ue,*P,*Yw,*Sfp,*sk,*zf,*fd1,*fd2,*sp,*sp2,
+    *pstat0,*pstatA,*pstatB,*pstatC,*out;
+};
+
+__global__ __launch_bounds__(256,4) void k_megasw(MP p, unsigned* bars){
+  __shared__ float sh[7920];
+  for (int u=blockIdx.x;u<2048;u+=NBLK){ __syncthreads(); st_scol(u,sh,p.x,p.A,p.pstat0); }
+  gbar(bars+0);
+  if (blockIdx.x<384) st_row64(blockIdx.x,sh,p.A,p.pstat0,p.norm1_g,p.norm1_b,p.X64,p.X64h);
+  gbar(bars+1);
+  for (int u=blockIdx.x;u<3072;u+=NBLK){ __syncthreads(); st_uezyw(u,sh,p.X64,p.X64h,p.query_w,p.query_sw,p.key_w,p.key_sw,p.value_w,p.value_sw,p.value_sb,p.proj_w,p.proj_sw,p.Zq,p.Zk,p.Yw,p.Ue); }
+  gbar(bars+2);
+  if (blockIdx.x<128) st_scores(blockIdx.x,sh,p.Zq,p.Zk,p.Ue,p.query_sw,p.query_sb,p.key_sw,p.key_sb,p.P);
+  gbar(bars+3);
+  if (blockIdx.x<528) st_sfsk(blockIdx.x,sh,p.x,p.P,p.Yw,p.proj_sw,p.value_sw,p.pstat0,p.norm1_g,p.norm1_b,p.Sfp,p.sk);
+  gbar(bars+4);
+  for (int u=blockIdx.x;u<2304;u+=NBLK){ __syncthreads(); st_f0sp(u,sh,p.Sfp,p.sk,p.x,p.P,p.X64,p.pstat0,p.norm1_g,p.norm1_b,p.proj_sw,p.value_sw,p.proj_sw,p.value_sb,p.proj_sb,p.zf,p.pstatA,p.sp); }
+  gbar(bars+5);
+  for (int u=blockIdx.x;u<2048;u+=NBLK){ __syncthreads(); st_field1(u,sh,p.sp,p.mw1,p.pstatA,p.attn_g,p.norm2_g,p.norm2_b,p.fd1,p.pstatB); }
+  gbar(bars+6);
+  st_colA1(blockIdx.x,sh,p.fd1,p.zf,p.pstatA,p.pstatB,p.attn_g,p.norm2_g,p.mng1,p.norm2_b,p.mnb1,p.msw1,p.msb1,p.A);
+  gbar(bars+7);
+  if (blockIdx.x<512) st_row32(blockIdx.x,sh,p.A,p.sp2);
+  gbar(bars+8);
+  for (int u=blockIdx.x;u<2048;u+=NBLK){ __syncthreads(); st_field2(u,sh,p.sp2,p.mw2,p.fd1,p.zf,p.pstatA,p.pstatB,p.attn_g,p.norm2_g,p.mng1,p.norm2_b,p.mnb1,p.msw1,p.msb1,p.fd2,p.pstatC); }
+  gbar(bars+9);
+  for (int u=blockIdx.x;u<2048;u+=NBLK){ st_final(u,p.zf,p.fd1,p.fd2,p.pstatA,p.pstatB,p.pstatC,p.attn_g,p.norm2_g,p.mng1,p.mng2,p.outg,p.attn_b,p.norm2_b,p.mnb1,p.msw1,p.msb1,p.mnb2,p.msw2,p.msb2,p.outb,p.out); }
+}
+
+__global__ __launch_bounds__(256) void k_scol(const float* x, float* A, float* pstat){
+  __shared__ float sh[4896];
+  st_scol(blockIdx.x, sh, x, A, pstat);
+}
+__global__ __launch_bounds__(256) void k_rowfft64(const float* A, const float* pstat0,
+    const float* n1g, const float* n1b, float* X64, float* X64h){
+  __shared__ float sh[7670];
+  st_row64(blockIdx.x + 128*blockIdx.y, sh, A, pstat0, n1g, n1b, X64, X64h);
+}
+__global__ __launch_bounds__(256) void k_UeZYw(const float* X64, const float* X64h,
+    const float* qw, const float* qsw, const float* kw, const float* ksw,
+    const float* value_w, const float* vsw, const float* vsb,
+    const float* proj_w, const float* psw,
+    float* Zq, float* Zk, float* Yw, float* Ue){
+  __shared__ float sh[4224];
+  st_uezyw(blockIdx.x, sh, X64, X64h, qw, qsw, kw, ksw, value_w, vsw, vsb, proj_w, psw, Zq, Zk, Yw, Ue);
+}
+__global__ __launch_bounds__(256) void k_scores2(const float* Zq, const float* Zk,
+    const float* Ue, const float* qsw, const float* qsb,
+    const float* ksw, const float* ksb, float* P){
+  __shared__ float sh[7920];
+  st_scores(blockIdx.x + 4*blockIdx.y + 64*blockIdx.z, sh, Zq, Zk, Ue, qsw, qsb, ksw, ksb, P);
+}
+__global__ __launch_bounds__(256) void k_SfSk(const float* x, const float* P, const float* Yw,
+    const float* pw, const float* vw, const float* pstat0, const float* n1g, const float* n1b,
+    float* Sfp, float* sk){
+  __shared__ float sh[4096];
+  st_sfsk(blockIdx.x, sh, x, P, Yw, pw, vw, pstat0, n1g, n1b, Sfp, sk);
+}
+__global__ __launch_bounds__(256) void k_f0sp(const float* Sfp, const float* sk, const float* x,
+    const float* P, const float* X64, const float* pstat0,
+    const float* n1g, const float* n1b, const float* pw, const float* vw,
+    const float* psw, const float* vsb, const float* psb,
+    float* zf, float* pstatA, float* sp){
+  __shared__ float sh[1616];
+  st_f0sp(blockIdx.x, sh, Sfp, sk, x, P, X64, pstat0, n1g, n1b, pw, vw, psw, vsb, psb, zf, pstatA, sp);
+}
+__global__ __launch_bounds__(256) void k_field1(const float* sp, const float* wm,
+    const float* pstatA, const float* ag, const float* n2g, const float* n2b,
+    float* fd1, float* pstatB){
+  __shared__ float sh[1616];
+  st_field1(blockIdx.x + 128*blockIdx.y, sh, sp, wm, pstatA, ag, n2g, n2b, fd1, pstatB);
+}
+__global__ __launch_bounds__(256) void k_colA1(const float* f1, const float* z,
+    const float* pstatA, const float* pstatB,
+    const float* ag, const float* n2g, const float* mng1, const float* n2b,
+    const float* mnb1, const float* msw1, const float* msb1, float* A){
+  __shared__ float sh[4896];
+  st_colA1(blockIdx.x, sh, f1, z, pstatA, pstatB, ag, n2g, mng1, n2b, mnb1, msw1, msb1, A);
+}
+__global__ __launch_bounds__(256) void k_rowfft32(const float* A, float* spec){
+  __shared__ float sh[2986];
+  st_row32(blockIdx.x + 128*blockIdx.y, sh, A, spec);
+}
+__global__ __launch_bounds__(256) void k_field2(const float* sp2, const float* wm,
+    const float* f1, const float* z, const float* pstatA, const float* pstatB,
+    const float* ag, const float* n2g, const float* mng1, const float* n2b,
+    const float* mnb1, const float* msw1, const float* msb1,
+    float* fd2, float* pstatC){
+  __shared__ float sh[1616];
+  st_field2(blockIdx.x + 128*blockIdx.y, sh, sp2, wm, f1, z, pstatA, pstatB, ag, n2g, mng1, n2b, mnb1, msw1, msb1, fd2, pstatC);
+}
+__global__ __launch_bounds__(256) void k_final2(const float* z, const float* f1, const float* f2,
+    const float* pstatA, const float* pstatB, const float* pstatC,
+    const float* ag, const float* n2g, const float* mng1, const float* mng2, const float* outg,
+    const float* ab, const float* n2b, const float* mnb1, const float* msw1, const float* msb1,
+    const float* mnb2, const float* msw2, const float* msb2, const float* outb, float* out){
+  st_final(blockIdx.x + 128*blockIdx.y, z, f1, f2, pstatA, pstatB, pstatC,
+           ag, n2g, mng1, mng2, outg, ab, n2b, mnb1, msw1, msb1, mnb2, msw2, msb2, outb, out);
 }
 
 extern "C" void kernel_launch(void* const* d_in, const int* in_sizes, int n_in,
@@ -862,22 +951,49 @@
   float* pstatA = ws + off; off += (size_t)128*16*2;
   float* pstatB = ws + off; off += (size_t)128*16*2;
   float* pstatC = ws + off; off += (size_t)128*16*5;
-
-  k_scol<<<2048,256,0,stream>>>(x, A, pstat0);
-  k_rowfft64<<<dim3(128,3),256,0,stream>>>(A, pstat0, norm1_g, norm1_b, X64, X64h);
-  k_UeZYw<<<3072,256,0,stream>>>(X64, X64h, query_w, query_sw, key_w, key_sw,
-      value_w, value_sw, value_sb, proj_w, proj_sw, Zq, Zk, Yw, Ue);
-  k_scores2<<<dim3(4,16,2),256,0,stream>>>(Zq, Zk, Ue, query_sw, query_sb, key_sw, key_sb, P);
-  k_SfSk<<<528,256,0,stream>>>(x, P, Yw, proj_sw, value_sw, pstat0, norm1_g, norm1_b, Sfp, sk);
-  k_f0sp<<<2304,256,0,stream>>>(Sfp, sk, x, P, X64, pstat0, norm1_g, norm1_b,
-      proj_sw, value_sw, proj_sw, value_sb, proj_sb, zf, pstatA, sp);
-  k_field1<<<dim3(128,16),256,0,stream>>>(sp, mw1, pstatA, attn_g, norm2_g, norm2_b, fd1, pstatB);
-  k_colA1<<<1024,256,0,stream>>>(fd1, zf, pstatA, pstatB, attn_g, norm2_g, mng1,
-      norm2_b, mnb1, msw1, msb1, A);
-  k_rowfft32<<<dim3(128,4),256,0,stream>>>(A, sp2);
-  k_field2<<<dim3(128,16),256,0,stream>>>(sp2, mw2, fd1, zf, pstatA, pstatB,
-      attn_g, norm2_g, mng1, norm2_b, mnb1, msw1, msb1, fd2, pstatC);
-  k_final2<<<dim3(128,16),256,0,stream>>>(zf, fd1, fd2, pstatA, pstatB, pstatC,
-      attn_g, norm2_g, mng1, mng2, outg, attn_b, norm2_b,
-      mnb1, msw1, msb1, mnb2, msw2, msb2, outb, out);
-}
+  unsigned* bars = (unsigned*)(ws + off); off += 16;
+
+  MP p;
+  p.x=x; p.key_w=key_w; p.key_sw=key_sw; p.key_sb=key_sb;
+  p.query_w=query_w; p.query_sw=query_sw; p.query_sb=query_sb;
+  p.value_w=value_w; p.value_sw=value_sw; p.value_sb=value_sb;
+  p.proj_w=proj_w; p.proj_sw=proj_sw; p.proj_sb=proj_sb;
+  p.norm1_g=norm1_g; p.norm1_b=norm1_b; p.attn_g=attn_g; p.attn_b=attn_b;
+  p.norm2_g=norm2_g; p.norm2_b=norm2_b;
+  p.mw1=mw1; p.msw1=msw1; p.msb1=msb1; p.mng1=mng1; p.mnb1=mnb1;
+  p.mw2=mw2; p.msw2=msw2; p.msb2=msb2; p.mng2=mng2; p.mnb2=mnb2;
+  p.outg=outg; p.outb=outb;
+  p.A=A; p.X64=X64; p.X64h=X64h; p.Zq=Zq; p.Zk=Zk; p.Ue=Ue; p.P=P; p.Yw=Yw;
+  p.Sfp=Sfp; p.sk=sk; p.zf=zf; p.fd1=fd1; p.fd2=fd2; p.sp=sp; p.sp2=sp2;
+  p.pstat0=pstat0; p.pstatA=pstatA; p.pstatB=pstatB; p.pstatC=pstatC; p.out=out;
+
+  static int mega_ok = -1;
+  if (mega_ok < 0){
+    int nb = 0;
+    hipError_t qe = hipOccupancyMaxActiveBlocksPerMultiprocessor(&nb, k_megasw, 256, 0);
+    mega_ok = (qe == hipSuccess && nb >= 4) ? 1 : 0;
+  }
+
+  if (mega_ok == 1){
+    hipMemsetAsync(bars, 0, 16*sizeof(unsigned), stream);
+    k_megasw<<<dim3(1024),dim3(256),0,stream>>>(p, bars);
+  } else {
+    k_scol<<<2048,256,0,stream>>>(x, A, pstat0);
+    k_rowfft64<<<dim3(128,3),256,0,stream>>>(A, pstat0, norm1_g, norm1_b, X64, X64h);
+    k_UeZYw<<<3072,256,0,stream>>>(X64, X64h, query_w, query_sw, key_w, key_sw,
+        value_w, value_sw, value_sb, proj_w, proj_sw, Zq, Zk, Yw, Ue);
+    k_scores2<<<dim3(4,16,2),256,0,stream>>>(Zq, Zk, Ue, query_sw, query_sb, key_sw, key_sb, P);
+    k_SfSk<<<528,256,0,stream>>>(x, P, Yw, proj_sw, value_sw, pstat0, norm1_g, norm1_b, Sfp, sk);
+    k_f0sp<<<2304,256,0,stream>>>(Sfp, sk, x, P, X64, pstat0, norm1_g, norm1_b,
+        proj_sw, value_sw, proj_sw, value_sb, proj_sb, zf, pstatA, sp);
+    k_field1<<<dim3(128,16),256,0,stream>>>(sp, mw1, pstatA, attn_g, norm2_g, norm2_b, fd1, pstatB);
+    k_colA1<<<1024,256,0,stream>>>(fd1, zf, pstatA, pstatB, attn_g, norm2_g, mng1,
+        norm2_b, mnb1, msw1, msb1, A);
+    k_rowfft32<<<dim3(128,4),256,0,stream>>>(A, sp2);
+    k_field2<<<dim3(128,16),256,0,stream>>>(sp2, mw2, fd1, zf, pstatA, pstatB,
+        attn_g, norm2_g, mng1, norm2_b, mnb1, msw1, msb1, fd2, pstatC);
+    k_final2<<<dim3(128,16),256,0,stream>>>(zf, fd1, fd2, pstatA, pstatB, pstatC,
+        attn_g, norm2_g, mng1, mng2, outg, attn_b, norm2_b,
+        mnb1, msw1, msb1, mnb2, msw2, msb2, outb, out);
+  }
+}
```

Result: slower. 277.4 us (+2.1%).
